# Performance work log

Hardware: AMD Instinct MI355X
Metric: run time of the kernel (lower is better)

Reference implementation:

```python
import jax, jax.numpy as jnp
import numpy as np

B = 32
NUM_CLASSES = 2


def _conv3d(x, w, b):
    # 3x3x3 'same' conv, NCDHW
    y = jax.lax.conv_general_dilated(x, w, (1, 1, 1), [(1, 1)] * 3,
                                     dimension_numbers=("NCDHW", "OIDHW", "NCDHW"))
    return y + b[None, :, None, None, None]


def _bn(x, g, b, axes, eps=1e-5):
    # training-mode batchnorm (biased variance), channel axis = 1
    m = jnp.mean(x, axes, keepdims=True)
    v = jnp.var(x, axes, keepdims=True)
    sh = [1] * x.ndim
    sh[1] = -1
    return (x - m) / jnp.sqrt(v + eps) * g.reshape(sh) + b.reshape(sh)


def _ln(x, g, b, eps=1e-6):
    m = jnp.mean(x, -1, keepdims=True)
    v = jnp.var(x, -1, keepdims=True)
    return (x - m) / jnp.sqrt(v + eps) * g + b


def _lin(x, w, b):
    return x @ w.T + b


def _conv1x1(x, w, b):
    # 1x1x1 Conv3d == channel-mixing linear
    return jnp.einsum("bcdhw,oc->bodhw", x, w) + b[None, :, None, None, None]


def _catnum(t, w, b, g, be, attr, out_attr):
    # Conv1d(attr->196, k=1) == Linear; BN1d over (batch, length); SiLU; tile channels
    t = _lin(t.reshape(t.shape[0], attr), w, b)               # [B,196]
    t = _bn(t[:, :, None], g, be, (0, 2))[:, :, 0]
    t = t * jax.nn.sigmoid(t)                                  # SiLU
    return jnp.broadcast_to(t.reshape(-1, 1, 4, 7, 7), (t.shape[0], out_attr, 4, 7, 7))


def _gcn(t, w, b):
    # all-pairs L1-distance affinity over CHANNELS (detached), then matmul + MLP + residual
    bsz, c = t.shape[0], t.shape[1]
    f = t.reshape(bsz, c, -1)                                  # [B,C,196]
    dist = jax.lax.stop_gradient(
        jnp.exp(-jnp.abs(f[:, :, None, :] - f[:, None, :, :]).sum(-1)))  # [B,C,C]
    out = jax.nn.relu(_lin(jnp.einsum("bij,bjn->bin", dist, f), w, b))
    return out.reshape(t.shape) + t


def _crossatt(img, text, e1_w, e1_b, e2_w, e2_b, f1_w, f1_b, f2_w, f2_b, f3_w, f3_b, f4_w, f4_b):
    # q/k/v each come from the SAME linear applied to the same input -> identical tensors
    iq = jax.nn.relu(_lin(img, e1_w, e1_b))                    # [B,128,196]
    tq = jax.nn.relu(_lin(text, e2_w, e2_b))                   # [B,45,196]
    att = lambda q, k: jax.nn.softmax(jnp.einsum("bik,bjk->bij", q, k), axis=-1)
    img_fea = att(iq, iq) @ iq
    text_fea = att(tq, tq) @ tq
    it_fea = att(iq, tq) @ tq
    ti_fea = att(tq, iq) @ iq
    return (_lin(img_fea, f1_w, f1_b) + _lin(it_fea, f3_w, f3_b) + img,
            _lin(text_fea, f2_w, f2_b) + _lin(ti_fea, f4_w, f4_b) + text)


def _cmsa(xf, w, b, fw, fb):
    # query=key=value (same conv applied thrice to same input)
    bsz, c, d, hh, ww = xf.shape
    q = jax.nn.relu(_conv1x1(xf, w, b)).reshape(bsz, c, -1)    # [B,173,196]
    A = jax.nn.softmax(jnp.einsum("bci,bcj->bij", q, q), axis=-1)  # [B,196,196]
    fea = jnp.einsum("bij,bcj->bci", A, q).reshape(bsz, c, d, hh, ww)
    return jax.nn.relu(_conv1x1(fea, fw, fb)) + xf


def _forward(x, oneHot, num, c1_w1, c1_b1, c1_g1, c1_be1, c1_w2, c1_b2, c1_g2, c1_be2,
             oh_w, oh_b, oh_g, oh_be, nm_w, nm_b, nm_g, nm_be,
             gm1_w, gm1_b, gm2_w, gm2_b, ln1_g, ln1_b, ln2_g, ln2_b,
             e1_w, e1_b, e2_w, e2_b, f1_w, f1_b, f2_w, f2_b, f3_w, f3_b, f4_w, f4_b,
             cm_w, cm_b, cmf_w, cmf_b, cls_w, cls_b):
    h = jax.nn.relu(_bn(_conv3d(x, c1_w1, c1_b1), c1_g1, c1_be1, (0, 2, 3, 4)))
    conv5 = jax.nn.relu(_bn(_conv3d(h, c1_w2, c1_b2), c1_g2, c1_be2, (0, 2, 3, 4)))  # [B,128,4,7,7]
    t_oh = _catnum(oneHot, oh_w, oh_b, oh_g, oh_be, 24, 30)    # [B,30,4,7,7]
    t_nm = _catnum(num, nm_w, nm_b, nm_g, nm_be, 11, 15)       # [B,15,4,7,7]
    text = jnp.concatenate([t_oh, t_nm], axis=1)               # [B,45,4,7,7]
    conv5 = _gcn(conv5, gm1_w, gm1_b)
    text = _gcn(text, gm2_w, gm2_b)
    bsz = x.shape[0]
    c5f = conv5.reshape(bsz, 128, 196)
    txf = text.reshape(bsz, 45, 196)
    ci, ct = _crossatt(_ln(c5f, ln1_g, ln1_b), _ln(txf, ln2_g, ln2_b),
                       e1_w, e1_b, e2_w, e2_b, f1_w, f1_b, f2_w, f2_b, f3_w, f3_b, f4_w, f4_b)
    feat = jnp.concatenate([(ci + c5f).reshape(bsz, 128, 4, 7, 7),
                            (ct + txf).reshape(bsz, 45, 4, 7, 7)], axis=1)  # [B,173,4,7,7]
    cmsa = _cmsa(feat, cm_w, cm_b, cmf_w, cmf_b)
    g1v = t_oh.reshape(bsz, 30, -1).sum(-1)
    g2v = t_nm.reshape(bsz, 15, -1).sum(-1)
    pcm = cmsa.reshape(bsz, 173, -1).sum(-1)
    return _lin(jnp.concatenate([g1v, g2v, pcm], axis=1), cls_w, cls_b)  # [B,num_classes]


def setup_inputs():
    key = jax.random.key(0)
    ks = iter(jax.random.split(key, 64))
    rn = lambda shape, s=0.02: jax.random.normal(next(ks), shape, jnp.float32) * s
    d = {}
    d["x"] = rn((B, 320, 4, 7, 7), 1.0)
    d["oneHot"] = (jax.random.uniform(next(ks), (B, 24)) > 0.5).astype(jnp.float32)
    d["num"] = rn((B, 11), 1.0)
    d["c1_w1"] = rn((128, 320, 3, 3, 3)); d["c1_b1"] = jnp.zeros(128)
    d["c1_g1"] = jnp.ones(128); d["c1_be1"] = jnp.zeros(128)
    d["c1_w2"] = rn((128, 128, 3, 3, 3)); d["c1_b2"] = jnp.zeros(128)
    d["c1_g2"] = jnp.ones(128); d["c1_be2"] = jnp.zeros(128)
    d["oh_w"] = rn((196, 24), 0.1); d["oh_b"] = jnp.zeros(196)
    d["oh_g"] = jnp.ones(196); d["oh_be"] = jnp.zeros(196)
    d["nm_w"] = rn((196, 11), 0.1); d["nm_b"] = jnp.zeros(196)
    d["nm_g"] = jnp.ones(196); d["nm_be"] = jnp.zeros(196)
    d["gm1_w"] = rn((196, 196), 0.05); d["gm1_b"] = jnp.zeros(196)
    d["gm2_w"] = rn((196, 196), 0.05); d["gm2_b"] = jnp.zeros(196)
    d["ln1_g"] = jnp.ones(196); d["ln1_b"] = jnp.zeros(196)
    d["ln2_g"] = jnp.ones(196); d["ln2_b"] = jnp.zeros(196)
    for n in ["e1", "e2", "f1", "f2", "f3", "f4"]:
        d[n + "_w"] = rn((196, 196), 0.05); d[n + "_b"] = jnp.zeros(196)
    d["cm_w"] = rn((173, 173), 0.05); d["cm_b"] = jnp.zeros(173)
    d["cmf_w"] = rn((173, 173), 0.05); d["cmf_b"] = jnp.zeros(173)
    d["cls_w"] = rn((NUM_CLASSES, 218), 0.05); d["cls_b"] = jnp.zeros(NUM_CLASSES)
    return d


def reference(x, oneHot, num, c1_w1, c1_b1, c1_g1, c1_be1, c1_w2, c1_b2, c1_g2, c1_be2,
              oh_w, oh_b, oh_g, oh_be, nm_w, nm_b, nm_g, nm_be,
              gm1_w, gm1_b, gm2_w, gm2_b, ln1_g, ln1_b, ln2_g, ln2_b,
              e1_w, e1_b, e2_w, e2_b, f1_w, f1_b, f2_w, f2_b, f3_w, f3_b, f4_w, f4_b,
              cm_w, cm_b, cmf_w, cmf_b, cls_w, cls_b):
    return _forward(x, oneHot, num, c1_w1, c1_b1, c1_g1, c1_be1, c1_w2, c1_b2, c1_g2, c1_be2,
                    oh_w, oh_b, oh_g, oh_be, nm_w, nm_b, nm_g, nm_be,
                    gm1_w, gm1_b, gm2_w, gm2_b, ln1_g, ln1_b, ln2_g, ln2_b,
                    e1_w, e1_b, e2_w, e2_b, f1_w, f1_b, f2_w, f2_b, f3_w, f3_b, f4_w, f4_b,
                    cm_w, cm_b, cmf_w, cmf_b, cls_w, cls_b)
```

## Files before the change

### kernel.cpp

```cpp
#include <hip/hip_runtime.h>
#include <hip/hip_bf16.h>


using bf16x8 = __attribute__((ext_vector_type(8))) short;
using f32x4  = __attribute__((ext_vector_type(4))) float;

typedef const __attribute__((address_space(1))) void gas_void;
typedef __attribute__((address_space(3))) void las_void;

__device__ __forceinline__ unsigned short f2bf(float f) {
    unsigned int u = __float_as_uint(f);
    u += 0x7FFFu + ((u >> 16) & 1u);
    return (unsigned short)(u >> 16);
}

__device__ __forceinline__ void d_wpack(const float* __restrict__ w,
                                        unsigned short* __restrict__ wp,
                                        int IC, int idx) {
    int nc = IC >> 3;
    if (idx >= 27 * 128 * nc) return;
    int c = idx % nc; int r = idx / nc; int oc = r & 127; int t = r >> 7;
    const float* ws = w + ((size_t)oc * IC + c * 8) * 27 + t;
    unsigned int o0 = f2bf(ws[0])   | ((unsigned int)f2bf(ws[27])  << 16);
    unsigned int o1 = f2bf(ws[54])  | ((unsigned int)f2bf(ws[81])  << 16);
    unsigned int o2 = f2bf(ws[108]) | ((unsigned int)f2bf(ws[135]) << 16);
    unsigned int o3 = f2bf(ws[162]) | ((unsigned int)f2bf(ws[189]) << 16);
    uint4 v; v.x = o0; v.y = o1; v.z = o2; v.w = o3;
    ((uint4*)wp)[idx] = v;
}

__device__ __forceinline__ void d_w173(const float* __restrict__ w,
                                       unsigned short* __restrict__ wb, int idx) {
    if (idx >= 176 * 192) return;
    int oc = idx / 192, c = idx - oc * 192;
    wb[idx] = (oc < 173 && c < 173) ? f2bf(w[(size_t)oc * 173 + c]) : (unsigned short)0;
}

__device__ __forceinline__ void d_wcat(const float* __restrict__ wA,
                                       const float* __restrict__ wB,
                                       unsigned short* __restrict__ outw, int idx) {
    if (idx >= 208 * 448) return;
    int n = idx / 448, k = idx - n * 448;
    unsigned short v = 0;
    if (n < 196) {
        if (k < 196) v = f2bf(wA[(size_t)n * 196 + k]);
        else if (k >= 224 && k < 420) v = f2bf(wB[(size_t)n * 196 + (k - 224)]);
    }
    outw[idx] = v;
}

__global__ void k_prep1(const float* __restrict__ c1w1, unsigned short* __restrict__ wp1,
                        const float* __restrict__ c1w2, unsigned short* __restrict__ wp2,
                        const float* __restrict__ x, unsigned short* __restrict__ xt1) {
    int blk = blockIdx.x, tid = threadIdx.x;
    if (blk < 540) { d_wpack(c1w1, wp1, 320, blk * 256 + tid); return; }
    blk -= 540;
    if (blk < 216) { d_wpack(c1w2, wp2, 128, blk * 256 + tid); return; }
    blk -= 216;
    int b = blk / 147, ib = blk - b * 147;
    const int tot = 5 * 208 * 36;
    int idx = ib * 256 + tid;
    if (idx >= tot) return;
    int g = idx / (208 * 36); int r2 = idx - g * (208 * 36);
    int s = r2 / 36, cp = r2 - s * 36;
    int cc = cp * 2;
    int ic = g * 64 + cc;
    unsigned int lo = 0, hi = 0;
    if (s < 196 && cc < 64 && ic < 320)         lo = f2bf(x[((size_t)b * 320 + ic) * 196 + s]);
    if (s < 196 && cc + 1 < 64 && ic + 1 < 320) hi = f2bf(x[((size_t)b * 320 + ic + 1) * 196 + s]);
    ((unsigned int*)xt1)[(size_t)b * tot + idx] = lo | (hi << 16);
}

__global__ void k_prep2(const float* __restrict__ cm_w, unsigned short* __restrict__ wcmb,
                        const float* __restrict__ cmf_w, unsigned short* __restrict__ wcmfb,
                        const float* __restrict__ gm1_w, unsigned short* __restrict__ gm1b,
                        float4* __restrict__ ftbz,
                        const float* __restrict__ gm2_w, const float* __restrict__ e1_w,
                        const float* __restrict__ e2_w, float* __restrict__ wT) {
    int blk = blockIdx.x, tid = threadIdx.x;
    if (blk < 132) { d_w173(cm_w, wcmb, blk * 256 + tid); return; }
    blk -= 132;
    if (blk < 132) { d_w173(cmf_w, wcmfb, blk * 256 + tid); return; }
    blk -= 132;
    if (blk < 182) {
        int idx = blk * 256 + tid;
        if (idx < 208 * 224) {
            int r = idx / 224, c = idx - r * 224;
            gm1b[idx] = (r < 196 && c < 196) ? f2bf(gm1_w[(size_t)r * 196 + c])
                                             : (unsigned short)0;
        }
        return;
    }
    blk -= 182;
    if (blk < 624) {
        int i = blk * 256 + tid;
        if (i < 159744) ftbz[i] = (float4){0.f, 0.f, 0.f, 0.f};
        return;
    }
    blk -= 624;
    {
        int m = blk / 196, i = blk - m * 196;
        const float* w = (m == 0) ? gm2_w : (m == 1) ? e1_w : e2_w;
        float* o = wT + (size_t)m * 38416;
        if (tid < 196) o[(size_t)i * 196 + tid] = w[(size_t)tid * 196 + i];
    }
}

__global__ void k_cattext(const float* __restrict__ oneHot, const float* __restrict__ num,
                          const float* __restrict__ ohw, const float* __restrict__ ohb,
                          const float* __restrict__ ohg, const float* __restrict__ ohbe,
                          const float* __restrict__ nmw, const float* __restrict__ nmb,
                          const float* __restrict__ nmg, const float* __restrict__ nmbe,
                          float* __restrict__ toh, float* __restrict__ tnm,
                          float* __restrict__ text, float* __restrict__ textT) {
    int blk = blockIdx.x;
    int lane = threadIdx.x;
    const int isOH = (blk < 196);
    const int j = isOH ? blk : blk - 196;
    const float* inp = isOH ? oneHot : num;
    const int A = isOH ? 24 : 11;
    const float* w = isOH ? ohw : nmw;
    const float* bias = isOH ? ohb : nmb;
    const float* g = isOH ? ohg : nmg;
    const float* be = isOH ? ohbe : nmbe;
    float v = 0.f;
    if (lane < 32) {
        v = bias[j];
        for (int k = 0; k < A; ++k) v += inp[lane * A + k] * w[j * A + k];
    }
    float s = (lane < 32) ? v : 0.f;
    float s2 = (lane < 32) ? v * v : 0.f;
    for (int m = 16; m; m >>= 1) { s += __shfl_xor(s, m, 32); s2 += __shfl_xor(s2, m, 32); }
    if (lane < 32) {
        float mean = s / 32.f;
        float var = s2 / 32.f - mean * mean;
        float rstd = rsqrtf(var + 1e-5f);
        float t = (v - mean) * rstd * g[j] + be[j];
        t = t / (1.f + expf(-t));
        int b = lane;
        if (isOH) {
            toh[b * 196 + j] = t;
            for (int c = 0; c < 30; ++c) {
                text[((size_t)(b * 45 + c)) * 196 + j] = t;
                textT[((size_t)(b * 196 + j)) * 45 + c] = t;
            }
        } else {
            tnm[b * 196 + j] = t;
            for (int c = 30; c < 45; ++c) {
                text[((size_t)(b * 45 + c)) * 196 + j] = t;
                textT[((size_t)(b * 196 + j)) * 45 + c] = t;
            }
        }
    }
}

__device__ __forceinline__ void d_dist_img(const float* __restrict__ f,
                                           const float* __restrict__ fT,
                                           unsigned short* __restrict__ distb,
                                           int bx, int b, int tid) {
    __shared__ float fi[4][196];
    const int i0 = bx * 4;
    for (int idx = tid; idx < 4 * 196; idx += 256) {
        int r = idx / 196, n = idx - r * 196;
        fi[r][n] = f[((size_t)(b * 128 + i0 + r)) * 196 + n];
    }
    __syncthreads();
    if (tid < 128) {
        const float* ft = fT + (size_t)b * 196 * 128 + tid;
        float a[4];
#pragma unroll
        for (int r = 0; r < 4; ++r) a[r] = 0.f;
#pragma unroll 4
        for (int n = 0; n < 196; ++n) {
            float v = ft[(size_t)n * 128];
#pragma unroll
            for (int r = 0; r < 4; ++r) a[r] += fabsf(fi[r][n] - v);
        }
#pragma unroll
        for (int r = 0; r < 4; ++r)
            distb[((size_t)(b * 128 + i0 + r)) * 128 + tid] = f2bf(expf(-a[r]));
    }
}

__device__ __forceinline__ void d_dist_txt(const float* __restrict__ f,
                                           const float* __restrict__ fT,
                                           float* __restrict__ dist,
                                           int bx, int b, int tid) {
    __shared__ float fi2[3][196];
    const int i0 = bx * 3;
    for (int idx = tid; idx < 3 * 196; idx += 256) {
        int r = idx / 196, n = idx - r * 196;
        fi2[r][n] = f[((size_t)(b * 45 + i0 + r)) * 196 + n];
    }
    __syncthreads();
    if (tid < 45) {
        const float* ft = fT + (size_t)b * 196 * 45 + tid;
        float a[3];
#pragma unroll
        for (int r = 0; r < 3; ++r) a[r] = 0.f;
#pragma unroll 4
        for (int n = 0; n < 196; ++n) {
            float v = ft[(size_t)n * 45];
#pragma unroll
            for (int r = 0; r < 3; ++r) a[r] += fabsf(fi2[r][n] - v);
        }
#pragma unroll
        for (int r = 0; r < 3; ++r)
            dist[((size_t)(b * 45 + i0 + r)) * 45 + tid] = expf(-a[r]);
    }
}

__global__ void k_dist_both(const float* __restrict__ fimg, const float* __restrict__ fTimg,
                            unsigned short* __restrict__ distb,
                            const float* __restrict__ ftxt, const float* __restrict__ fTtxt,
                            float* __restrict__ dist2) {
    int blk = blockIdx.x, tid = threadIdx.x;
    if (blk < 1024) d_dist_img(fimg, fTimg, distb, blk & 31, blk >> 5, tid);
    else { int r = blk - 1024; d_dist_txt(ftxt, fTtxt, dist2, r % 15, r / 15, tid); }
}

__global__ void k_prep3(float4* __restrict__ tqz,
                        const float* __restrict__ f1w, const float* __restrict__ f3w,
                        unsigned short* __restrict__ wcI,
                        const float* __restrict__ f4w, const float* __restrict__ f2w,
                        unsigned short* __restrict__ wcT) {
    int blk = blockIdx.x, tid = threadIdx.x;
    if (blk < 208) {
        int i = blk * 256 + tid;
        if (i < 53248) tqz[i] = (float4){0.f, 0.f, 0.f, 0.f};
        return;
    }
    blk -= 208;
    if (blk < 364) { d_wcat(f1w, f3w, wcI, blk * 256 + tid); return; }
    blk -= 364;
    d_wcat(f4w, f2w, wcT, blk * 256 + tid);
}

__global__ void k_prep4(float4* __restrict__ zA, float4* __restrict__ zB) {
    int blk = blockIdx.x, tid = threadIdx.x;
    if (blk < 1344) {
        int i = blk * 256 + tid;
        if (i < 344064) zA[i] = (float4){0.f, 0.f, 0.f, 0.f};
        return;
    }
    blk -= 1344;
    int i = blk * 256 + tid;
    if (i < 319488) zB[i] = (float4){0.f, 0.f, 0.f, 0.f};
}

template <int IC, int G, int NT, int NH>
__global__ __launch_bounds__(256, 3) void k_convchunk4(
    const unsigned short* __restrict__ xt, const unsigned short* __restrict__ wp,
    float* __restrict__ part) {
    __shared__ unsigned short xs[208 * 72];
    __shared__ char bbuf[2][NT * 2048];
    const int tid = threadIdx.x;
    const int bx = blockIdx.x, b = blockIdx.y;
    const int mh = bx & 1;
    const int nh = (bx >> 1) % NH;
    const int g  = (bx >> 1) / NH;
    const int w = tid >> 6, l = tid & 63;

    {
        const bf16x8* s8 = (const bf16x8*)(xt + ((size_t)b * G + g) * (208 * 72));
        bf16x8* d8 = (bf16x8*)xs;
        for (int c = tid; c < 208 * 72 / 8; c += 256) d8[c] = s8[c];
    }

    const char* wslice = (const char*)wp +
                         ((size_t)(nh * NT * 16) * IC + (size_t)g * 64) * 2;
    auto stageB = [&](int t) {
        char* dst = &bbuf[t & 1][w * (NT * 512)];
        const char* wt_ = wslice + (size_t)t * 128 * IC * 2;
#pragma unroll
        for (int c = 0; c < NT / 2; ++c) {
            int q = w * (NT * 512) + c * 1024 + l * 16;
            int row = q >> 7, col = q & 127;
            int scol = col ^ ((row & 7) << 4);
            gas_void* src = (gas_void*)(wt_ + (size_t)row * IC * 2 + scol);
            __builtin_amdgcn_global_load_lds(src, (las_void*)(dst + c * 1024),
                                             16, 0, 0);
        }
    };

    const int lane = tid & 63;
    const int a = lane & 15, kg = lane >> 4;

    int md[2], mhh[2], mw[2];
#pragma unroll
    for (int i = 0; i < 2; ++i) {
        int m = (mh * 8 + (tid >> 6) * 2 + i) * 16 + a;
        md[i] = m / 49; int rr = m - md[i] * 49;
        mhh[i] = rr / 7; mw[i] = rr - mhh[i] * 7;
    }

    f32x4 acc[2][NT];
#pragma unroll
    for (int i = 0; i < 2; ++i)
#pragma unroll
        for (int nt = 0; nt < NT; ++nt) acc[i][nt] = (f32x4){0.f, 0.f, 0.f, 0.f};

    const bf16x8 zv = {0, 0, 0, 0, 0, 0, 0, 0};

    stageB(0);
    __syncthreads();

    for (int t = 0; t < 27; ++t) {
        if (t < 26) stageB(t + 1);
        const int kd = t / 9, kh = (t / 3) % 3, kw = t % 3;
        int rsrc[2]; bool ok[2];
#pragma unroll
        for (int i = 0; i < 2; ++i) {
            int d2 = md[i] + kd - 1, h2 = mhh[i] + kh - 1, w2 = mw[i] + kw - 1;
            ok[i] = ((unsigned)d2 < 4u) & ((unsigned)h2 < 7u) & ((unsigned)w2 < 7u);
            rsrc[i] = ok[i] ? (d2 * 49 + h2 * 7 + w2) : 0;
        }
        bf16x8 A[2][2];
#pragma unroll
        for (int kk = 0; kk < 2; ++kk)
#pragma unroll
            for (int i = 0; i < 2; ++i) {
                bf16x8 v = *(const bf16x8*)(xs + rsrc[i] * 72 + kk * 32 + kg * 8);
                A[kk][i] = ok[i] ? v : zv;
            }
        const char* bb = &bbuf[t & 1][0];
#pragma unroll
        for (int kk = 0; kk < 2; ++kk)
#pragma unroll
            for (int nt = 0; nt < NT; ++nt) {
                int row = nt * 16 + a;
                int cb = (kk * 64 + kg * 16) ^ ((row & 7) << 4);
                bf16x8 B = *(const bf16x8*)(bb + row * 128 + cb);
#pragma unroll
                for (int i = 0; i < 2; ++i)
                    acc[i][nt] = __builtin_amdgcn_mfma_f32_16x16x32_bf16(
                        A[kk][i], B, acc[i][nt], 0, 0, 0);
            }
        __syncthreads();
    }

    float* dst = part + ((size_t)g * 32 + b) * (128 * 196);
#pragma unroll
    for (int i = 0; i < 2; ++i) {
        int m0 = (mh * 8 + (tid >> 6) * 2 + i) * 16 + kg * 4;
        if (m0 < 196) {
#pragma unroll
            for (int nt = 0; nt < NT; ++nt) {
                int oc = nh * NT * 16 + nt * 16 + a;
                *(f32x4*)(dst + (size_t)oc * 196 + m0) = acc[i][nt];
            }
        }
    }
}

template <int G, int C>
__global__ void k_reduce_stats(const float* __restrict__ part, float* __restrict__ y,
                               float* __restrict__ pst) {
    const int ch = blockIdx.x, b = blockIdx.y;
    const int tid = threadIdx.x;
    __shared__ float r1[4], r2[4];
    float v = 0.f;
    if (tid < 196) {
#pragma unroll
        for (int g = 0; g < G; ++g)
            v += part[((size_t)(g * 32 + b) * C + ch) * 196 + tid];
        y[((size_t)b * C + ch) * 196 + tid] = v;
    }
    float s = v, s2 = v * v;
    for (int sh = 32; sh; sh >>= 1) { s += __shfl_xor(s, sh); s2 += __shfl_xor(s2, sh); }
    if ((tid & 63) == 0) { r1[tid >> 6] = s; r2[tid >> 6] = s2; }
    __syncthreads();
    if (tid == 0) {
        pst[(ch * 32 + b) * 2]     = r1[0] + r1[1] + r1[2] + r1[3];
        pst[(ch * 32 + b) * 2 + 1] = r2[0] + r2[1] + r2[2] + r2[3];
    }
}

__global__ void k_bn_apply2(float* __restrict__ y, const float* __restrict__ pst,
                            const float* __restrict__ g, const float* __restrict__ be,
                            float* __restrict__ fT, unsigned short* __restrict__ fTb,
                            unsigned short* __restrict__ xtc, int C) {
    int idx = blockIdx.x;
    int ch = idx % C, b = idx / C;
    int s = threadIdx.x;
    float S = 0.f, S2 = 0.f;
    for (int b2 = 0; b2 < 32; ++b2) {
        S += pst[(ch * 32 + b2) * 2];
        S2 += pst[(ch * 32 + b2) * 2 + 1];
    }
    if (s < 196) {
        float m = S / 6272.f;
        float r = rsqrtf(S2 / 6272.f - m * m + 1e-5f);
        float v = y[(size_t)idx * 196 + s];
        float o = fmaxf((v - m) * r * g[ch] + be[ch], 0.f);
        y[(size_t)idx * 196 + s] = o;
        if (fT) fT[((size_t)b * 196 + s) * C + ch] = o;
        if (fTb) fTb[((size_t)b * 208 + s) * C + ch] = f2bf(o);
        if (xtc) {
            int G = C >> 6, gch = ch >> 6, cc = ch & 63;
            xtc[(((size_t)b * G + gch) * 208 + s) * 72 + cc] = f2bf(o);
        }
    }
}

template <int MROWS, int MTILES, int KP, int KK, int EPI, int NS>
__global__ __launch_bounds__(256, 2) void k_bgemm(
    const unsigned short* __restrict__ Ab, size_t ABS,
    const unsigned short* __restrict__ Bb, size_t BBS,
    const float* __restrict__ bias,
    unsigned short* __restrict__ p0, unsigned short* __restrict__ p1,
    const float* __restrict__ resid, float* __restrict__ outf) {
    constexpr int KPS = KP + 8;
    __shared__ unsigned short xsA[64 * KPS];
    __shared__ char bbuf[2][208 * 64];
    const int tid = threadIdx.x, bx = blockIdx.x, b = blockIdx.y;
    const int wv = tid >> 6, lane = tid & 63, a = lane & 15, kg = lane >> 4;
    const int nh = bx % NS, mg = bx / NS;
    const int NT0 = (NS == 1) ? 0 : nh * 7;
    const int NTN = (NS == 1) ? 13 : ((nh == 0) ? 7 : 6);

    const unsigned short* Abase = Ab + (size_t)b * ABS;
    {
        const int rowu = KP / 2;
        for (int i = tid; i < 64 * rowu; i += 256) {
            int r = i / rowu, cu = i - r * rowu;
            int gr = mg * 64 + r; if (gr > MROWS - 1) gr = MROWS - 1;
            unsigned int v = ((const unsigned int*)(Abase + (size_t)gr * KP))[cu];
            *(unsigned int*)&xsA[r * KPS + cu * 2] = v;
        }
    }
    const char* Bbase = (const char*)(Bb + (size_t)b * BBS);
    auto stageB = [&](int kk) {
        char* dst0 = &bbuf[kk & 1][0];
        const int cnt = NTN * 64;
#pragma unroll
        for (int c = 0; c < 4; ++c) {
            int idx = tid + c * 256;
            if (idx < cnt) {
                int lrow = idx >> 2, u = idx & 3;
                int grow = NT0 * 16 + lrow;
                gas_void* src = (gas_void*)(Bbase + (size_t)grow * (KP * 2) +
                                            kk * 64 + u * 16);
                __builtin_amdgcn_global_load_lds(src, (las_void*)(dst0 + (size_t)idx * 16),
                                                 16, 0, 0);
            }
        }
    };

    int mt = mg * 4 + wv; if (mt > MTILES - 1) mt = MTILES - 1;
    const int arow = mt * 16 + a - mg * 64;

    f32x4 acc[13];
#pragma unroll
    for (int nt = 0; nt < 13; ++nt) acc[nt] = (f32x4){0.f, 0.f, 0.f, 0.f};

    stageB(0);
    __syncthreads();
    for (int kk = 0; kk < KK; ++kk) {
        if (kk + 1 < KK) stageB(kk + 1);
        bf16x8 Af = *(const bf16x8*)&xsA[arow * KPS + kk * 32 + kg * 8];
        const char* bb = &bbuf[kk & 1][0];
#pragma unroll
        for (int nt = 0; nt < 13; ++nt) {
            if (nt >= NT0 && nt < NT0 + NTN) {
                bf16x8 Bf = *(const bf16x8*)(bb + ((nt - NT0) * 16 + a) * 64 + kg * 16);
                acc[nt] = __builtin_amdgcn_mfma_f32_16x16x32_bf16(Af, Bf, acc[nt], 0, 0, 0);
            }
        }
        __syncthreads();
    }

    const int mbase = mt * 16 + kg * 4;
    if (EPI == 0) {
#pragma unroll
        for (int nt = 0; nt < 13; ++nt) {
            if (nt < NT0 || nt >= NT0 + NTN) continue;
            int col = nt * 16 + a;
            if (col < 196) {
#pragma unroll
                for (int j = 0; j < 4; ++j) {
                    int row = mbase + j;
                    if (row < 173) {
                        unsigned short h = f2bf(fmaxf(acc[nt][j] + bias[row], 0.f));
                        p0[((size_t)b * 176 + row) * 224 + col] = h;
                        p1[((size_t)b * 208 + col) * 192 + row] = h;
                    }
                }
            }
        }
    } else if (EPI == 1) {
#pragma unroll
        for (int j = 0; j < 4; ++j) {
            int row = mbase + j;
            float m = -3.4e38f;
#pragma unroll
            for (int nt = 0; nt < 13; ++nt) {
                int col = nt * 16 + a;
                float s = (col < 196) ? acc[nt][j] : -3.4e38f;
                m = fmaxf(m, s);
            }
            for (int msk = 1; msk < 16; msk <<= 1) m = fmaxf(m, __shfl_xor(m, msk));
            float e[13]; float sum = 0.f;
#pragma unroll
            for (int nt = 0; nt < 13; ++nt) {
                int col = nt * 16 + a;
                float v = (col < 196) ? expf(acc[nt][j] - m) : 0.f;
                e[nt] = v; sum += v;
            }
            for (int msk = 1; msk < 16; msk <<= 1) sum += __shfl_xor(sum, msk);
            float inv = 1.f / sum;
            if (row < 196) {
#pragma unroll
                for (int nt = 0; nt < 13; ++nt) {
                    int col = nt * 16 + a;
                    p0[((size_t)b * 208 + row) * 224 + col] = f2bf(e[nt] * inv);
                }
            }
        }
    } else if (EPI == 2) {
#pragma unroll
        for (int nt = 0; nt < 13; ++nt) {
            if (nt < NT0 || nt >= NT0 + NTN) continue;
            int col = nt * 16 + a;
#pragma unroll
            for (int j = 0; j < 4; ++j) {
                int row = mbase + j;
                if (row < 173)
                    p0[((size_t)b * 208 + col) * 192 + row] = f2bf(acc[nt][j]);
            }
        }
    } else if (EPI == 3) {
#pragma unroll
        for (int nt = 0; nt < 13; ++nt) {
            if (nt < NT0 || nt >= NT0 + NTN) continue;
            int col = nt * 16 + a;
            if (col < 196) {
#pragma unroll
                for (int j = 0; j < 4; ++j) {
                    int row = mbase + j;
                    if (row < 173) {
                        size_t rr = ((size_t)b * 173 + row) * 196 + col;
                        outf[rr] = fmaxf(acc[nt][j] + bias[row], 0.f) + resid[rr];
                    }
                }
            }
        }
    } else {
#pragma unroll
        for (int nt = 0; nt < 13; ++nt) {
            if (nt < NT0 || nt >= NT0 + NTN) continue;
            int col = nt * 16 + a;
            if (col < 196) {
#pragma unroll
                for (int j = 0; j < 4; ++j) {
                    int row = mbase + j;
                    size_t rr = ((size_t)b * 128 + row) * 196 + col;
                    outf[rr] = fmaxf(acc[nt][j] + bias[col], 0.f) + resid[rr];
                }
            }
        }
    }
}

__global__ __launch_bounds__(256, 2) void k_gcnpair(
    const unsigned short* __restrict__ distb, const unsigned short* __restrict__ fTb,
    unsigned short* __restrict__ tmpb,
    const float* __restrict__ d2, const float* __restrict__ t1,
    const float* __restrict__ gm2T, const float* __restrict__ gm2b,
    float* __restrict__ t3) {
    __shared__ unsigned short xsA[64 * 136];
    __shared__ char bbuf[2][208 * 64];
    __shared__ float ds[3][45];
    __shared__ float ts[3][196];
    const int tid = threadIdx.x, b = blockIdx.y;
    int bx = blockIdx.x;
    if (bx < 4) {
        const int wv = tid >> 6, lane = tid & 63, a = lane & 15, kg = lane >> 4;
        const int nh = bx % 2, mg = bx / 2;
        const int NT0 = nh * 7, NTN = (nh == 0) ? 7 : 6;
        const unsigned short* Abase = distb + (size_t)b * 128 * 128;
        for (int i = tid; i < 64 * 64; i += 256) {
            int r = i / 64, cu = i - r * 64;
            int gr = mg * 64 + r;
            unsigned int v = ((const unsigned int*)(Abase + (size_t)gr * 128))[cu];
            *(unsigned int*)&xsA[r * 136 + cu * 2] = v;
        }
        const char* Bbase = (const char*)(fTb + (size_t)b * 208 * 128);
        auto stageB = [&](int kk) {
            char* dst0 = &bbuf[kk & 1][0];
            const int cnt = NTN * 64;
#pragma unroll
            for (int c = 0; c < 4; ++c) {
                int idx = tid + c * 256;
                if (idx < cnt) {
                    int lrow = idx >> 2, u = idx & 3;
                    int grow = NT0 * 16 + lrow;
                    gas_void* src = (gas_void*)(Bbase + (size_t)grow * 256 +
                                                kk * 64 + u * 16);
                    __builtin_amdgcn_global_load_lds(src,
                        (las_void*)(dst0 + (size_t)idx * 16), 16, 0, 0);
                }
            }
        };
        int mt = mg * 4 + wv;
        const int arow = mt * 16 + a - mg * 64;
        f32x4 acc[13];
#pragma unroll
        for (int nt = 0; nt < 13; ++nt) acc[nt] = (f32x4){0.f, 0.f, 0.f, 0.f};
        stageB(0);
        __syncthreads();
        for (int kk = 0; kk < 4; ++kk) {
            if (kk + 1 < 4) stageB(kk + 1);
            bf16x8 Af = *(const bf16x8*)&xsA[arow * 136 + kk * 32 + kg * 8];
            const char* bb = &bbuf[kk & 1][0];
#pragma unroll
            for (int nt = 0; nt < 13; ++nt) {
                if (nt >= NT0 && nt < NT0 + NTN) {
                    bf16x8 Bf = *(const bf16x8*)(bb + ((nt - NT0) * 16 + a) * 64 + kg * 16);
                    acc[nt] = __builtin_amdgcn_mfma_f32_16x16x32_bf16(Af, Bf, acc[nt], 0, 0, 0);
                }
            }
            __syncthreads();
        }
        const int mbase = mt * 16 + kg * 4;
#pragma unroll
        for (int nt = 0; nt < 13; ++nt) {
            if (nt < NT0 || nt >= NT0 + NTN) continue;
            int col = nt * 16 + a;
#pragma unroll
            for (int j = 0; j < 4; ++j) {
                int row = mbase + j;
                unsigned short h = (col < 196) ? f2bf(acc[nt][j]) : (unsigned short)0;
                tmpb[((size_t)b * 128 + row) * 224 + col] = h;
            }
        }
    } else {
        const int i0 = (bx - 4) * 3;
        for (int idx = tid; idx < 3 * 45; idx += 256) {
            int r = idx / 45, j = idx - r * 45;
            ds[r][j] = d2[((size_t)(b * 45 + i0 + r)) * 45 + j];
        }
        __syncthreads();
        if (tid < 196) {
            float a[3];
#pragma unroll
            for (int r = 0; r < 3; ++r) a[r] = 0.f;
#pragma unroll 4
            for (int j = 0; j < 45; ++j) {
                float v = t1[((size_t)b * 45 + j) * 196 + tid];
#pragma unroll
                for (int r = 0; r < 3; ++r) a[r] += ds[r][j] * v;
            }
#pragma unroll
            for (int r = 0; r < 3; ++r) ts[r][tid] = a[r];
        }
        __syncthreads();
        if (tid < 196) {
            float a[3];
            float bi = gm2b[tid];
#pragma unroll
            for (int r = 0; r < 3; ++r) a[r] = bi;
#pragma unroll 4
            for (int n = 0; n < 196; ++n) {
                float wv = gm2T[(size_t)n * 196 + tid];
#pragma unroll
                for (int r = 0; r < 3; ++r) a[r] += ts[r][n] * wv;
            }
#pragma unroll
            for (int r = 0; r < 3; ++r) {
                size_t rr = ((size_t)(b * 45 + i0 + r)) * 196 + tid;
                t3[rr] = fmaxf(a[r], 0.f) + t1[rr];
            }
        }
    }
}

struct AG {
    const unsigned short* Ab; unsigned long ABS;
    const unsigned short* Bb; unsigned long BBS;
    const float* biasA; const float* biasB;
    const float* lnres; const float* res2;
    unsigned short* p0; unsigned long p0rs, p0bs;
    float* feat; unsigned short* ftb; int cbase;
    int MROWS; int MTILES;
};

template <int KPA, int KPB, int KK, int EPI, int STAGEA, int NS>
__global__ __launch_bounds__(256, 2) void k_agemm2(AG pa, AG pc, int split) {
    constexpr int KPS = KPA + 8;
    __shared__ unsigned short xsA[STAGEA ? 64 * KPS : 64];
    __shared__ char bbuf[2][208 * 64];
    const AG P = (blockIdx.x < split) ? pa : pc;
    const int bx = (blockIdx.x < split) ? blockIdx.x : blockIdx.x - split;
    const int tid = threadIdx.x, b = blockIdx.y;
    const int wv = tid >> 6, lane = tid & 63, a = lane & 15, kg = lane >> 4;
    const int nh = bx % NS, mg = bx / NS;
    const int NT0 = (NS == 1) ? 0 : nh * 7;
    const int NTN = (NS == 1) ? 13 : ((nh == 0) ? 7 : 6);
    const int MROWS = P.MROWS, MTILES = P.MTILES;

    const unsigned short* Abase = P.Ab + (size_t)b * P.ABS;
    if (STAGEA) {
        const int rowu = KPA / 2;
        for (int i = tid; i < 64 * rowu; i += 256) {
            int r = i / rowu, cu = i - r * rowu;
            int gr = mg * 64 + r; if (gr > MROWS - 1) gr = MROWS - 1;
            unsigned int v = ((const unsigned int*)(Abase + (size_t)gr * KPA))[cu];
            *(unsigned int*)&xsA[r * KPS + cu * 2] = v;
        }
    }
    const char* Bbase = (const char*)(P.Bb + (size_t)b * P.BBS);
    auto stageB = [&](int kk) {
        char* dst0 = &bbuf[kk & 1][0];
        const int cnt = NTN * 64;
#pragma unroll
        for (int c = 0; c < 4; ++c) {
            int idx = tid + c * 256;
            if (idx < cnt) {
                int lrow = idx >> 2, u = idx & 3;
                int grow = NT0 * 16 + lrow;
                gas_void* src = (gas_void*)(Bbase + (size_t)grow * (KPB * 2) +
                                            kk * 64 + u * 16);
                __builtin_amdgcn_global_load_lds(src, (las_void*)(dst0 + (size_t)idx * 16),
                                                 16, 0, 0);
            }
        }
    };

    int mt = mg * 4 + wv; if (mt > MTILES - 1) mt = MTILES - 1;

    f32x4 acc[13];
#pragma unroll
    for (int nt = 0; nt < 13; ++nt) acc[nt] = (f32x4){0.f, 0.f, 0.f, 0.f};

    stageB(0);
    __syncthreads();
    for (int kk = 0; kk < KK; ++kk) {
        if (kk + 1 < KK) stageB(kk + 1);
        bf16x8 Af;
        if (STAGEA) {
            int arow = mt * 16 + a - mg * 64;
            Af = *(const bf16x8*)&xsA[arow * KPS + kk * 32 + kg * 8];
        } else {
            int gr = mt * 16 + a; if (gr > MROWS - 1) gr = MROWS - 1;
            Af = *(const bf16x8*)(Abase + (size_t)gr * KPA + kk * 32 + kg * 8);
        }
        const char* bb = &bbuf[kk & 1][0];
#pragma unroll
        for (int nt = 0; nt < 13; ++nt) {
            if (nt >= NT0 && nt < NT0 + NTN) {
                bf16x8 Bf = *(const bf16x8*)(bb + ((nt - NT0) * 16 + a) * 64 + kg * 16);
                acc[nt] = __builtin_amdgcn_mfma_f32_16x16x32_bf16(Af, Bf, acc[nt], 0, 0, 0);
            }
        }
        __syncthreads();
    }

    const int mbase = mt * 16 + kg * 4;
    if (EPI == 5) {
#pragma unroll
        for (int j = 0; j < 4; ++j) {
            int row = mbase + j;
            float mA = -3.4e38f, mB = -3.4e38f;
#pragma unroll
            for (int nt = 0; nt < 8; ++nt) mA = fmaxf(mA, acc[nt][j]);
#pragma unroll
            for (int nt = 8; nt < 13; ++nt) {
                int col = nt * 16 + a;
                float s = (col < 173) ? acc[nt][j] : -3.4e38f;
                mB = fmaxf(mB, s);
            }
            for (int msk = 1; msk < 16; msk <<= 1) {
                mA = fmaxf(mA, __shfl_xor(mA, msk));
                mB = fmaxf(mB, __shfl_xor(mB, msk));
            }
            float eA[8], eB[5];
            float sA = 0.f, sB = 0.f;
#pragma unroll
            for (int nt = 0; nt < 8; ++nt) { eA[nt] = expf(acc[nt][j] - mA); sA += eA[nt]; }
#pragma unroll
            for (int nt = 8; nt < 13; ++nt) {
                int col = nt * 16 + a;
                float v = (col < 173) ? expf(acc[nt][j] - mB) : 0.f;
                eB[nt - 8] = v; sB += v;
            }
            for (int msk = 1; msk < 16; msk <<= 1) {
                sA += __shfl_xor(sA, msk);
                sB += __shfl_xor(sB, msk);
            }
            float iA = 1.f / sA, iB = 1.f / sB;
            if (row < MROWS) {
#pragma unroll
                for (int nt = 0; nt < 12; ++nt) {
                    int col = nt * 16 + a;
                    float v = (nt < 8) ? eA[nt] * iA
                                       : ((col < 173) ? eB[nt - 8] * iB : 0.f);
                    P.p0[(size_t)b * P.p0bs + (size_t)row * P.p0rs + col] = f2bf(v);
                }
            }
        }
    } else {
#pragma unroll
        for (int nt = 0; nt < 13; ++nt) {
            if (nt < NT0 || nt >= NT0 + NTN) continue;
            int col = nt * 16 + a;
            if (col < 196) {
#pragma unroll
                for (int j = 0; j < 4; ++j) {
                    int row = mbase + j;
                    if (row < MROWS) {
                        size_t rr = ((size_t)b * MROWS + row) * 196 + col;
                        float v = acc[nt][j] + P.biasA[col] + P.biasB[col] +
                                  P.lnres[rr] + P.res2[rr];
                        P.feat[((size_t)b * 173 + P.cbase + row) * 196 + col] = v;
                        P.ftb[((size_t)(b * 208 + col)) * 192 + P.cbase + row] = f2bf(v);
                    }
                }
            }
        }
    }
}

struct PVP { const unsigned short* P; unsigned long Pbs;
             unsigned short* F; unsigned long Fbs; int MROWS; int MTILES; };

__global__ __launch_bounds__(256, 2) void k_pv2(
    PVP pa, PVP pc, int split,
    const unsigned short* __restrict__ V1, unsigned long V1bs,
    const unsigned short* __restrict__ V2, unsigned long V2bs) {
    constexpr int KPS = 200;
    __shared__ unsigned short xsA[64 * KPS];
    __shared__ char bbuf[2][208 * 64];
    const PVP P = (blockIdx.x < split) ? pa : pc;
    const int bx = (blockIdx.x < split) ? blockIdx.x : blockIdx.x - split;
    const int tid = threadIdx.x, b = blockIdx.y;
    const int wv = tid >> 6, lane = tid & 63, a = lane & 15, kg = lane >> 4;
    const int nh = bx % 2, mg = bx / 2;
    const int NT0 = nh * 7, NTN = (nh == 0) ? 7 : 6;
    const int MROWS = P.MROWS, MTILES = P.MTILES;

    const unsigned short* Abase = P.P + (size_t)b * P.Pbs;
    {
        for (int i = tid; i < 64 * 96; i += 256) {
            int r = i / 96, cu = i - r * 96;
            int gr = mg * 64 + r; if (gr > MROWS - 1) gr = MROWS - 1;
            unsigned int v = ((const unsigned int*)(Abase + (size_t)gr * 192))[cu];
            *(unsigned int*)&xsA[r * KPS + cu * 2] = v;
        }
    }
    int mt = mg * 4 + wv; if (mt > MTILES - 1) mt = MTILES - 1;
    const int arow = mt * 16 + a - mg * 64;
    const int mbase = mt * 16 + kg * 4;

    auto run = [&](const unsigned short* Vb, size_t Vbs_, int KPB, int KK,
                   int AOFFe, int outoff) {
        f32x4 acc[13];
#pragma unroll
        for (int nt = 0; nt < 13; ++nt) acc[nt] = (f32x4){0.f, 0.f, 0.f, 0.f};
        const char* Bbase = (const char*)(Vb + (size_t)b * Vbs_);
        auto stageB = [&](int kk) {
            char* dst0 = &bbuf[kk & 1][0];
            const int cnt = NTN * 64;
#pragma unroll
            for (int c = 0; c < 4; ++c) {
                int idx = tid + c * 256;
                if (idx < cnt) {
                    int lrow = idx >> 2, u = idx & 3;
                    int grow = NT0 * 16 + lrow;
                    gas_void* src = (gas_void*)(Bbase + (size_t)grow * (KPB * 2) +
                                                kk * 64 + u * 16);
                    __builtin_amdgcn_global_load_lds(src,
                        (las_void*)(dst0 + (size_t)idx * 16), 16, 0, 0);
                }
            }
        };
        stageB(0);
        __syncthreads();
        for (int kk = 0; kk < KK; ++kk) {
            if (kk + 1 < KK) stageB(kk + 1);
            bf16x8 Af = *(const bf16x8*)&xsA[arow * KPS + AOFFe + kk * 32 + kg * 8];
            const char* bb = &bbuf[kk & 1][0];
#pragma unroll
            for (int nt = 0; nt < 13; ++nt) {
                if (nt >= NT0 && nt < NT0 + NTN) {
                    bf16x8 Bf = *(const bf16x8*)(bb + ((nt - NT0) * 16 + a) * 64 + kg * 16);
                    acc[nt] = __builtin_amdgcn_mfma_f32_16x16x32_bf16(Af, Bf, acc[nt], 0, 0, 0);
                }
            }
            __syncthreads();
        }
#pragma unroll
        for (int nt = 0; nt < 13; ++nt) {
            if (nt < NT0 || nt >= NT0 + NTN) continue;
            int col = nt * 16 + a;
#pragma unroll
            for (int j = 0; j < 4; ++j) {
                int row = mbase + j;
                if (row < MROWS) {
                    unsigned short h = (col < 196) ? f2bf(acc[nt][j]) : (unsigned short)0;
                    P.F[(size_t)b * P.Fbs + (size_t)row * 448 + outoff + col] = h;
                }
            }
        }
        if (nh == 1) {
            int col = 208 + a;
#pragma unroll
            for (int j = 0; j < 4; ++j) {
                int row = mbase + j;
                if (row < MROWS)
                    P.F[(size_t)b * P.Fbs + (size_t)row * 448 + outoff + col] = 0;
            }
        }
    };
    run(V1, V1bs, 128, 4, 0, 0);
    run(V2, V2bs, 64, 2, 128, 224);
}

template <int R, int ROWS, int KOFF, int TS>
__device__ __forceinline__ void d_lnlin(const float* __restrict__ x,
                                        const float* __restrict__ g,
                                        const float* __restrict__ be,
                                        const float* __restrict__ eT,
                                        const float* __restrict__ eb,
                                        float* __restrict__ lnout,
                                        unsigned short* __restrict__ kcat,
                                        unsigned short* __restrict__ tbuf,
                                        int bx, int b) {
    __shared__ float ls[ROWS][196];
    const int i0 = bx * ROWS;
    const int tid = threadIdx.x;
    const int wv = tid >> 6, lane = tid & 63;
    for (int idx = tid; idx < ROWS * 196; idx += 256) {
        int r = idx / 196, n = idx - r * 196;
        ls[r][n] = x[((size_t)(b * R + i0 + r)) * 196 + n];
    }
    __syncthreads();
    for (int k = 0;; ++k) {
        int r = wv + 4 * k;
        if (r >= ROWS) break;
        float s = 0.f, s2 = 0.f;
        for (int j = lane; j < 196; j += 64) { float v = ls[r][j]; s += v; s2 += v * v; }
        for (int sh = 32; sh; sh >>= 1) { s += __shfl_xor(s, sh); s2 += __shfl_xor(s2, sh); }
        float mean = s / 196.f;
        float var = s2 / 196.f - mean * mean;
        float rstd = rsqrtf(var + 1e-6f);
        size_t rowo = ((size_t)(b * R + i0 + r)) * 196;
        for (int j = lane; j < 196; j += 64) {
            float l = (ls[r][j] - mean) * rstd * g[j] + be[j];
            ls[r][j] = l;
            lnout[rowo + j] = l;
        }
    }
    __syncthreads();
    if (tid < 224) {
        float a[ROWS];
        if (tid < 196) {
            float bi = eb[tid];
#pragma unroll
            for (int r = 0; r < ROWS; ++r) a[r] = bi;
#pragma unroll 4
            for (int n = 0; n < 196; ++n) {
                float ev = eT[(size_t)n * 196 + tid];
#pragma unroll
                for (int r = 0; r < ROWS; ++r) a[r] += ls[r][n] * ev;
            }
        }
#pragma unroll
        for (int r = 0; r < ROWS; ++r) {
            unsigned short h = 0;
            if (tid < 196) h = f2bf(fmaxf(a[r], 0.f));
            kcat[((size_t)(b * 208 + KOFF + i0 + r)) * 224 + tid] = h;
            if (tid < 196) tbuf[((size_t)(b * 208 + tid)) * TS + (i0 + r)] = h;
        }
    }
}

__global__ void k_lnlin_both(const float* __restrict__ ximg, const float* __restrict__ g1,
                             const float* __restrict__ b1, const float* __restrict__ e1T,
                             const float* __restrict__ e1b, float* __restrict__ ln1out,
                             const float* __restrict__ xtxt, const float* __restrict__ g2,
                             const float* __restrict__ b2, const float* __restrict__ e2T,
                             const float* __restrict__ e2b, float* __restrict__ ln2out,
                             unsigned short* __restrict__ kcat,
                             unsigned short* __restrict__ iqT,
                             unsigned short* __restrict__ tqT) {
    int blk = blockIdx.x;
    if (blk < 1024)
        d_lnlin<128, 4, 0, 128>(ximg, g1, b1, e1T, e1b, ln1out, kcat, iqT,
                                blk & 31, blk >> 5);
    else {
        int r = blk - 1024;
        d_lnlin<45, 3, 128, 64>(xtxt, g2, b2, e2T, e2b, ln2out, kcat, tqT,
                                r % 15, r / 15);
    }
}

__global__ void k_finale(const float* __restrict__ toh, const float* __restrict__ tnm,
                         const float* __restrict__ cms, const float* __restrict__ cls_w,
                         const float* __restrict__ cls_b, float* __restrict__ out) {
    int b = blockIdx.x;
    __shared__ float pcm[173];
    __shared__ float r1[4], r2[4];
    int tid = threadIdx.x;
    float a = (tid < 196) ? toh[b * 196 + tid] : 0.f;
    float c = (tid < 196) ? tnm[b * 196 + tid] : 0.f;
    for (int sh = 32; sh; sh >>= 1) { a += __shfl_xor(a, sh); c += __shfl_xor(c, sh); }
    if ((tid & 63) == 0) { r1[tid >> 6] = a; r2[tid >> 6] = c; }
    if (tid < 173) {
        float s = 0.f;
        const float* p = &cms[((size_t)b * 173 + tid) * 196];
        for (int n = 0; n < 196; ++n) s += p[n];
        pcm[tid] = s;
    }
    __syncthreads();
    if (tid < 2) {
        float soh = r1[0] + r1[1] + r1[2] + r1[3];
        float snm = r2[0] + r2[1] + r2[2] + r2[3];
        const float* wrow = &cls_w[tid * 218];
        float acc = cls_b[tid];
        float w1 = 0.f, w2 = 0.f;
        for (int k = 0; k < 30; ++k) w1 += wrow[k];
        for (int k = 30; k < 45; ++k) w2 += wrow[k];
        acc += soh * w1 + snm * w2;
        for (int k = 0; k < 173; ++k) acc += wrow[45 + k] * pcm[k];
        out[b * 2 + tid] = acc;
    }
}

extern "C" void kernel_launch(void* const* d_in, const int* in_sizes, int n_in,
                              void* d_out, int out_size, void* d_ws, size_t ws_size,
                              hipStream_t stream) {
    const float* x      = (const float*)d_in[0];
    const float* oneHot = (const float*)d_in[1];
    const float* num    = (const float*)d_in[2];
    const float* c1_w1  = (const float*)d_in[3];
    const float* c1_g1  = (const float*)d_in[5];
    const float* c1_be1 = (const float*)d_in[6];
    const float* c1_w2  = (const float*)d_in[7];
    const float* c1_g2  = (const float*)d_in[9];
    const float* c1_be2 = (const float*)d_in[10];
    const float* oh_w   = (const float*)d_in[11];
    const float* oh_b   = (const float*)d_in[12];
    const float* oh_g   = (const float*)d_in[13];
    const float* oh_be  = (const float*)d_in[14];
    const float* nm_w   = (const float*)d_in[15];
    const float* nm_b   = (const float*)d_in[16];
    const float* nm_g   = (const float*)d_in[17];
    const float* nm_be  = (const float*)d_in[18];
    const float* gm1_w  = (const float*)d_in[19];
    const float* gm1_b  = (const float*)d_in[20];
    const float* gm2_w  = (const float*)d_in[21];
    const float* gm2_b  = (const float*)d_in[22];
    const float* ln1_g  = (const float*)d_in[23];
    const float* ln1_b  = (const float*)d_in[24];
    const float* ln2_g  = (const float*)d_in[25];
    const float* ln2_b  = (const float*)d_in[26];
    const float* e1_w   = (const float*)d_in[27];
    const float* e1_b   = (const float*)d_in[28];
    const float* e2_w   = (const float*)d_in[29];
    const float* e2_b   = (const float*)d_in[30];
    const float* f1_w   = (const float*)d_in[31];
    const float* f1_b   = (const float*)d_in[32];
    const float* f2_w   = (const float*)d_in[33];
    const float* f2_b   = (const float*)d_in[34];
    const float* f3_w   = (const float*)d_in[35];
    const float* f3_b   = (const float*)d_in[36];
    const float* f4_w   = (const float*)d_in[37];
    const float* f4_b   = (const float*)d_in[38];
    const float* cm_w   = (const float*)d_in[39];
    const float* cm_b   = (const float*)d_in[40];
    const float* cmf_w  = (const float*)d_in[41];
    const float* cmf_b  = (const float*)d_in[42];
    const float* cls_w  = (const float*)d_in[43];
    const float* cls_b  = (const float*)d_in[44];
    float* out = (float*)d_out;
    float* W = (float*)d_ws;

    const size_t L = 802816;
    const size_t T = 282240;
    const size_t F3 = 1085056;
    const size_t o_A    = 0;
    const size_t o_B    = L;
    const size_t o_C    = 2 * L;
    const size_t o_Kcat = 3 * L;
    const size_t o_iqT  = o_Kcat + 745472;
    const size_t o_t1   = 4 * L + T;
    const size_t o_t3   = 4 * L + 2 * T;
    const size_t o_ln2  = 4 * L + 3 * T;
    const size_t o_toh  = 4 * L + 4 * T;
    const size_t o_tnm  = o_toh + 6272;
    const size_t o_st   = o_tnm + 6272;
    const size_t o_wT   = o_st + 1024;
    const size_t o_feat = o_wT + 8 * 38416;
    const size_t o_q    = o_feat + F3;
    const size_t o_Fimg = o_q;
    const size_t o_dd   = o_q + F3;
    const size_t o_db   = o_dd;
    const size_t o_d2   = o_dd + 524288;
    const size_t o_gm1b = o_dd + 589088;
    const size_t o_fTb  = o_dd + 612384;
    const size_t o_tqT  = o_dd;
    const size_t o_wcI  = o_dd + 212992;
    const size_t o_wcT  = o_wcI + 46592;
    const size_t o_pbf  = o_dd;
    const size_t o_qbf  = o_dd + 745472;
    const size_t o_Ftxt = o_qbf;
    const size_t o_wcm  = o_qbf + 630784;
    const size_t o_wcmf = o_wcm + 16896;
    const size_t o_ftb  = o_wcmf + 16896;
    const size_t o_tr   = o_ftb + 638976;
    const size_t o_Pimg = o_tr;
    const size_t o_Ptxt = o_tr + 393216;
    const size_t o_qtb  = o_tr;
    const size_t o_ps   = 10158208;
    const size_t o_xt1 = o_dd;
    const size_t o_xt2 = o_xt1 + 1198080;
    const size_t o_wp1 = o_xt2 + 479232;
    const size_t o_wp2 = o_wp1 + 552960;

    float* part = W + 3 * L;
    unsigned short* xt1 = (unsigned short*)(W + o_xt1);
    unsigned short* xt2 = (unsigned short*)(W + o_xt2);
    unsigned short* wp1 = (unsigned short*)(W + o_wp1);
    unsigned short* wp2 = (unsigned short*)(W + o_wp2);
    unsigned short* kcatb = (unsigned short*)(W + o_Kcat);
    unsigned short* iqTb = (unsigned short*)(W + o_iqT);
    unsigned short* tqTb = (unsigned short*)(W + o_tqT);
    unsigned short* wcatI = (unsigned short*)(W + o_wcI);
    unsigned short* wcatT = (unsigned short*)(W + o_wcT);
    unsigned short* Fimg = (unsigned short*)(W + o_Fimg);
    unsigned short* Ftxt = (unsigned short*)(W + o_Ftxt);
    unsigned short* Pimg = (unsigned short*)(W + o_Pimg);
    unsigned short* Ptxt = (unsigned short*)(W + o_Ptxt);
    unsigned short* ftb = (unsigned short*)(W + o_ftb);
    unsigned short* qtb = (unsigned short*)(W + o_qtb);
    unsigned short* feab = (unsigned short*)(W + o_qtb + 638976);
    unsigned short* qbf = (unsigned short*)(W + o_qbf);
    unsigned short* wcmb = (unsigned short*)(W + o_wcm);
    unsigned short* wcmfb = (unsigned short*)(W + o_wcmf);
    unsigned short* pbf = (unsigned short*)(W + o_pbf);
    unsigned short* distb = (unsigned short*)(W + o_db);
    unsigned short* gm1b = (unsigned short*)(W + o_gm1b);
    unsigned short* fTb = (unsigned short*)(W + o_fTb);
    unsigned short* tmpb = (unsigned short*)(W + o_A);
    float* gm2T = W + o_wT + 0 * 38416;
    float* e1T  = W + o_wT + 1 * 38416;
    float* e2T  = W + o_wT + 2 * 38416;

    k_prep1<<<5460, 256, 0, stream>>>(c1_w1, wp1, c1_w2, wp2, x, xt1);

    k_convchunk4<320, 5, 4, 2><<<dim3(20, 32), 256, 0, stream>>>(xt1, wp1, part);
    k_reduce_stats<5, 128><<<dim3(128, 32), 256, 0, stream>>>(part, W + o_A, W + o_ps);
    k_bn_apply2<<<4096, 256, 0, stream>>>(W + o_A, W + o_ps, c1_g1, c1_be1,
                                          nullptr, nullptr, xt2, 128);

    k_convchunk4<128, 2, 2, 4><<<dim3(16, 32), 256, 0, stream>>>(xt2, wp2, part);
    k_reduce_stats<2, 128><<<dim3(128, 32), 256, 0, stream>>>(part, W + o_B,
                                                              W + o_ps + 8192);
    k_bn_apply2<<<4096, 256, 0, stream>>>(W + o_B, W + o_ps + 8192, c1_g2, c1_be2,
                                          W + o_tr, fTb, nullptr, 128);

    k_prep2<<<1658, 256, 0, stream>>>(cm_w, wcmb, cmf_w, wcmfb, gm1_w, gm1b,
                                      (float4*)(W + o_ftb), gm2_w, e1_w, e2_w, W + o_wT);

    k_cattext<<<392, 64, 0, stream>>>(oneHot, num, oh_w, oh_b, oh_g, oh_be,
                                      nm_w, nm_b, nm_g, nm_be,
                                      W + o_toh, W + o_tnm, W + o_t1, W + o_tr + L);

    k_dist_both<<<1504, 256, 0, stream>>>(W + o_B, W + o_tr, distb,
                                          W + o_t1, W + o_tr + L, W + o_d2);

    k_gcnpair<<<dim3(19, 32), 256, 0, stream>>>(distb, fTb, tmpb,
                                                W + o_d2, W + o_t1, gm2T, gm2_b,
                                                W + o_t3);

    k_bgemm<128, 8, 224, 7, 8, 2><<<dim3(4, 32), 256, 0, stream>>>(
        tmpb, (size_t)128 * 224, gm1b, 0, gm1_b,
        nullptr, nullptr, W + o_B, W + o_C);

    k_prep3<<<936, 256, 0, stream>>>((float4*)(W + o_tqT), f1_w, f3_w, wcatI,
                                     f4_w, f2_w, wcatT);

    k_lnlin_both<<<1504, 256, 0, stream>>>(W + o_C, ln1_g, ln1_b, e1T, e1_b, W + o_B,
                                           W + o_t3, ln2_g, ln2_b, e2T, e2_b, W + o_ln2,
                                           kcatb, iqTb, tqTb);

    {
        AG a{}, c{};
        a.Ab = kcatb; a.ABS = 208 * 224; a.Bb = kcatb; a.BBS = 208 * 224;
        a.p0 = Pimg; a.p0rs = 192; a.p0bs = (unsigned long)128 * 192;
        a.MROWS = 128; a.MTILES = 8;
        c = a;
        c.Ab = kcatb + 128 * 224; c.p0 = Ptxt; c.p0bs = (unsigned long)48 * 192;
        c.MROWS = 45; c.MTILES = 3;
        k_agemm2<224, 224, 7, 5, 1, 1><<<dim3(3, 32), 256, 0, stream>>>(a, c, 2);
    }

    {
        PVP a{Pimg, (unsigned long)128 * 192, Fimg, (unsigned long)128 * 448, 128, 8};
        PVP c{Ptxt, (unsigned long)48 * 192, Ftxt, (unsigned long)48 * 448, 45, 3};
        k_pv2<<<dim3(6, 32), 256, 0, stream>>>(a, c, 4, iqTb, (unsigned long)208 * 128,
                                               tqTb, (unsigned long)208 * 64);
    }

    {
        AG a{}, c{};
        a.Ab = Fimg; a.ABS = (unsigned long)128 * 448; a.Bb = wcatI; a.BBS = 0;
        a.biasA = f1_b; a.biasB = f3_b; a.lnres = W + o_B; a.res2 = W + o_C;
        a.feat = W + o_feat; a.ftb = ftb; a.cbase = 0; a.MROWS = 128; a.MTILES = 8;
        c = a;
        c.Ab = Ftxt; c.ABS = (unsigned long)48 * 448; c.Bb = wcatT;
        c.biasA = f2_b; c.biasB = f4_b; c.lnres = W + o_ln2; c.res2 = W + o_t3;
        c.cbase = 128; c.MROWS = 45; c.MTILES = 3;
        k_agemm2<448, 448, 14, 4, 0, 2><<<dim3(6, 32), 256, 0, stream>>>(a, c, 4);
    }

    k_prep4<<<2592, 256, 0, stream>>>((float4*)(W + o_pbf), (float4*)(W + o_qtb));

    k_bgemm<176, 11, 192, 6, 0, 2><<<dim3(6, 32), 256, 0, stream>>>(
        wcmb, 0, ftb, (size_t)208 * 192, cm_b, qbf, qtb, nullptr, nullptr);
    k_bgemm<208, 13, 192, 6, 1, 1><<<dim3(4, 32), 256, 0, stream>>>(
        qtb, (size_t)208 * 192, qtb, (size_t)208 * 192, nullptr, pbf, nullptr,
        nullptr, nullptr);
    k_bgemm<176, 11, 224, 7, 2, 2><<<dim3(6, 32), 256, 0, stream>>>(
        qbf, (size_t)176 * 224, pbf, (size_t)208 * 224, nullptr, feab, nullptr,
        nullptr, nullptr);
    k_bgemm<176, 11, 192, 6, 3, 2><<<dim3(6, 32), 256, 0, stream>>>(
        wcmfb, 0, feab, (size_t)208 * 192, cmf_b, nullptr, nullptr,
        W + o_feat, W + o_q);

    k_finale<<<32, 256, 0, stream>>>(W + o_toh, W + o_tnm, W + o_q, cls_w, cls_b, out);
}
```

Measured before the change: 317.9 us.

## Fuse attention score/softmax with PV GEMM and merge small prep kernels

Replaces the separate score GEMM (k_agemm2 with softmax epilogue) and PV kernel (k_pv2) with a single k_attn kernel. It keeps the softmax probabilities in LDS instead of writing them to global memory and reading them back. It also folds k_cattext into k_prep2 and the gcn final GEMM plus k_prep3 into one k_gcnfin launch, which cuts launch count and inter-kernel gaps. The risk is that k_attn uses only 96 blocks with no N-split, so parallelism per launch drops.

```diff
diff --git a/kernel.cpp b/kernel.cpp
--- a/kernel.cpp
+++ b/kernel.cpp
@@ -47,6 +47,54 @@
         else if (k >= 224 && k < 420) v = f2bf(wB[(size_t)n * 196 + (k - 224)]);
     }
     outw[idx] = v;
+}
+
+__device__ __forceinline__ void d_cattext(
+    int idx, int lane,
+    const float* __restrict__ oneHot, const float* __restrict__ num,
+    const float* __restrict__ ohw, const float* __restrict__ ohb,
+    const float* __restrict__ ohg, const float* __restrict__ ohbe,
+    const float* __restrict__ nmw, const float* __restrict__ nmb,
+    const float* __restrict__ nmg, const float* __restrict__ nmbe,
+    float* __restrict__ toh, float* __restrict__ tnm,
+    float* __restrict__ text, float* __restrict__ textT) {
+    const int isOH = (idx < 196);
+    const int j = isOH ? idx : idx - 196;
+    const float* inp = isOH ? oneHot : num;
+    const int A = isOH ? 24 : 11;
+    const float* w = isOH ? ohw : nmw;
+    const float* bias = isOH ? ohb : nmb;
+    const float* g = isOH ? ohg : nmg;
+    const float* be = isOH ? ohbe : nmbe;
+    float v = 0.f;
+    if (lane < 32) {
+        v = bias[j];
+        for (int k = 0; k < A; ++k) v += inp[lane * A + k] * w[j * A + k];
+    }
+    float s = (lane < 32) ? v : 0.f;
+    float s2 = (lane < 32) ? v * v : 0.f;
+    for (int m = 16; m; m >>= 1) { s += __shfl_xor(s, m, 32); s2 += __shfl_xor(s2, m, 32); }
+    if (lane < 32) {
+        float mean = s / 32.f;
+        float var = s2 / 32.f - mean * mean;
+        float rstd = rsqrtf(var + 1e-5f);
+        float t = (v - mean) * rstd * g[j] + be[j];
+        t = t / (1.f + expf(-t));
+        int b = lane;
+        if (isOH) {
+            toh[b * 196 + j] = t;
+            for (int c = 0; c < 30; ++c) {
+                text[((size_t)(b * 45 + c)) * 196 + j] = t;
+                textT[((size_t)(b * 196 + j)) * 45 + c] = t;
+            }
+        } else {
+            tnm[b * 196 + j] = t;
+            for (int c = 30; c < 45; ++c) {
+                text[((size_t)(b * 45 + c)) * 196 + j] = t;
+                textT[((size_t)(b * 196 + j)) * 45 + c] = t;
+            }
+        }
+    }
 }
 
 __global__ void k_prep1(const float* __restrict__ c1w1, unsigned short* __restrict__ wp1,
@@ -76,7 +124,14 @@
                         const float* __restrict__ gm1_w, unsigned short* __restrict__ gm1b,
                         float4* __restrict__ ftbz,
                         const float* __restrict__ gm2_w, const float* __restrict__ e1_w,
-                        const float* __restrict__ e2_w, float* __restrict__ wT) {
+                        const float* __restrict__ e2_w, float* __restrict__ wT,
+                        const float* __restrict__ oneHot, const float* __restrict__ num,
+                        const float* __restrict__ ohw, const float* __restrict__ ohb,
+                        const float* __restrict__ ohg, const float* __restrict__ ohbe,
+                        const float* __restrict__ nmw, const float* __restrict__ nmb,
+                        const float* __restrict__ nmg, const float* __restrict__ nmbe,
+                        float* __restrict__ toh, float* __restrict__ tnm,
+                        float* __restrict__ text, float* __restrict__ textT) {
     int blk = blockIdx.x, tid = threadIdx.x;
     if (blk < 132) { d_w173(cm_w, wcmb, blk * 256 + tid); return; }
     blk -= 132;
@@ -98,59 +153,19 @@
         return;
     }
     blk -= 624;
-    {
+    if (blk < 588) {
         int m = blk / 196, i = blk - m * 196;
         const float* w = (m == 0) ? gm2_w : (m == 1) ? e1_w : e2_w;
         float* o = wT + (size_t)m * 38416;
         if (tid < 196) o[(size_t)i * 196 + tid] = w[(size_t)tid * 196 + i];
-    }
-}
-
-__global__ void k_cattext(const float* __restrict__ oneHot, const float* __restrict__ num,
-                          const float* __restrict__ ohw, const float* __restrict__ ohb,
-                          const float* __restrict__ ohg, const float* __restrict__ ohbe,
-                          const float* __restrict__ nmw, const float* __restrict__ nmb,
-                          const float* __restrict__ nmg, const float* __restrict__ nmbe,
-                          float* __restrict__ toh, float* __restrict__ tnm,
-                          float* __restrict__ text, float* __restrict__ textT) {
-    int blk = blockIdx.x;
-    int lane = threadIdx.x;
-    const int isOH = (blk < 196);
-    const int j = isOH ? blk : blk - 196;
-    const float* inp = isOH ? oneHot : num;
-    const int A = isOH ? 24 : 11;
-    const float* w = isOH ? ohw : nmw;
-    const float* bias = isOH ? ohb : nmb;
-    const float* g = isOH ? ohg : nmg;
-    const float* be = isOH ? ohbe : nmbe;
-    float v = 0.f;
-    if (lane < 32) {
-        v = bias[j];
-        for (int k = 0; k < A; ++k) v += inp[lane * A + k] * w[j * A + k];
-    }
-    float s = (lane < 32) ? v : 0.f;
-    float s2 = (lane < 32) ? v * v : 0.f;
-    for (int m = 16; m; m >>= 1) { s += __shfl_xor(s, m, 32); s2 += __shfl_xor(s2, m, 32); }
-    if (lane < 32) {
-        float mean = s / 32.f;
-        float var = s2 / 32.f - mean * mean;
-        float rstd = rsqrtf(var + 1e-5f);
-        float t = (v - mean) * rstd * g[j] + be[j];
-        t = t / (1.f + expf(-t));
-        int b = lane;
-        if (isOH) {
-            toh[b * 196 + j] = t;
-            for (int c = 0; c < 30; ++c) {
-                text[((size_t)(b * 45 + c)) * 196 + j] = t;
-                textT[((size_t)(b * 196 + j)) * 45 + c] = t;
-            }
-        } else {
-            tnm[b * 196 + j] = t;
-            for (int c = 30; c < 45; ++c) {
-                text[((size_t)(b * 45 + c)) * 196 + j] = t;
-                textT[((size_t)(b * 196 + j)) * 45 + c] = t;
-            }
-        }
+        return;
+    }
+    blk -= 588;
+    {
+        int idx = blk * 4 + (tid >> 6);
+        if (idx < 392)
+            d_cattext(idx, tid & 63, oneHot, num, ohw, ohb, ohg, ohbe,
+                      nmw, nmb, nmg, nmbe, toh, tnm, text, textT);
     }
 }
 
@@ -217,23 +232,6 @@
     int blk = blockIdx.x, tid = threadIdx.x;
     if (blk < 1024) d_dist_img(fimg, fTimg, distb, blk & 31, blk >> 5, tid);
     else { int r = blk - 1024; d_dist_txt(ftxt, fTtxt, dist2, r % 15, r / 15, tid); }
-}
-
-__global__ void k_prep3(float4* __restrict__ tqz,
-                        const float* __restrict__ f1w, const float* __restrict__ f3w,
-                        unsigned short* __restrict__ wcI,
-                        const float* __restrict__ f4w, const float* __restrict__ f2w,
-                        unsigned short* __restrict__ wcT) {
-    int blk = blockIdx.x, tid = threadIdx.x;
-    if (blk < 208) {
-        int i = blk * 256 + tid;
-        if (i < 53248) tqz[i] = (float4){0.f, 0.f, 0.f, 0.f};
-        return;
-    }
-    blk -= 208;
-    if (blk < 364) { d_wcat(f1w, f3w, wcI, blk * 256 + tid); return; }
-    blk -= 364;
-    d_wcat(f4w, f2w, wcT, blk * 256 + tid);
 }
 
 __global__ void k_prep4(float4* __restrict__ zA, float4* __restrict__ zB) {
@@ -529,7 +527,7 @@
                     p0[((size_t)b * 208 + col) * 192 + row] = f2bf(acc[nt][j]);
             }
         }
-    } else if (EPI == 3) {
+    } else {
 #pragma unroll
         for (int nt = 0; nt < 13; ++nt) {
             if (nt < NT0 || nt >= NT0 + NTN) continue;
@@ -542,20 +540,6 @@
                         size_t rr = ((size_t)b * 173 + row) * 196 + col;
                         outf[rr] = fmaxf(acc[nt][j] + bias[row], 0.f) + resid[rr];
                     }
-                }
-            }
-        }
-    } else {
-#pragma unroll
-        for (int nt = 0; nt < 13; ++nt) {
-            if (nt < NT0 || nt >= NT0 + NTN) continue;
-            int col = nt * 16 + a;
-            if (col < 196) {
-#pragma unroll
-                for (int j = 0; j < 4; ++j) {
-                    int row = mbase + j;
-                    size_t rr = ((size_t)b * 128 + row) * 196 + col;
-                    outf[rr] = fmaxf(acc[nt][j] + bias[col], 0.f) + resid[rr];
                 }
             }
         }
@@ -675,21 +659,268 @@
     }
 }
 
+__global__ __launch_bounds__(256, 2) void k_gcnfin(
+    const unsigned short* __restrict__ tmpb, const unsigned short* __restrict__ gm1b,
+    const float* __restrict__ gm1bias, const float* __restrict__ resid,
+    float* __restrict__ outf,
+    float4* __restrict__ tqz,
+    const float* __restrict__ f1w, const float* __restrict__ f3w,
+    unsigned short* __restrict__ wcI,
+    const float* __restrict__ f4w, const float* __restrict__ f2w,
+    unsigned short* __restrict__ wcT) {
+    __shared__ unsigned short xsA[64 * 232];
+    __shared__ char bbuf[2][208 * 64];
+    const int tid = threadIdx.x;
+    int blk = blockIdx.x;
+    if (blk < 128) {
+        const int b = blk >> 2, bx = blk & 3;
+        const int wv = tid >> 6, lane = tid & 63, a = lane & 15, kg = lane >> 4;
+        const int nh = bx & 1, mg = bx >> 1;
+        const int NT0 = nh * 7, NTN = (nh == 0) ? 7 : 6;
+        const unsigned short* Abase = tmpb + (size_t)b * (128 * 224);
+        for (int i = tid; i < 64 * 112; i += 256) {
+            int r = i / 112, cu = i - r * 112;
+            int gr = mg * 64 + r;
+            unsigned int v = ((const unsigned int*)(Abase + (size_t)gr * 224))[cu];
+            *(unsigned int*)&xsA[r * 232 + cu * 2] = v;
+        }
+        auto stageB = [&](int kk) {
+            char* dst0 = &bbuf[kk & 1][0];
+            const int cnt = NTN * 64;
+#pragma unroll
+            for (int c = 0; c < 4; ++c) {
+                int idx = tid + c * 256;
+                if (idx < cnt) {
+                    int lrow = idx >> 2, u = idx & 3;
+                    int grow = NT0 * 16 + lrow;
+                    gas_void* src = (gas_void*)((const char*)gm1b + (size_t)grow * 448 +
+                                                kk * 64 + u * 16);
+                    __builtin_amdgcn_global_load_lds(src,
+                        (las_void*)(dst0 + (size_t)idx * 16), 16, 0, 0);
+                }
+            }
+        };
+        int mt = mg * 4 + wv;
+        const int arow = mt * 16 + a - mg * 64;
+        f32x4 acc[13];
+#pragma unroll
+        for (int nt = 0; nt < 13; ++nt) acc[nt] = (f32x4){0.f, 0.f, 0.f, 0.f};
+        stageB(0);
+        __syncthreads();
+        for (int kk = 0; kk < 7; ++kk) {
+            if (kk + 1 < 7) stageB(kk + 1);
+            bf16x8 Af = *(const bf16x8*)&xsA[arow * 232 + kk * 32 + kg * 8];
+            const char* bb = &bbuf[kk & 1][0];
+#pragma unroll
+            for (int nt = 0; nt < 13; ++nt) {
+                if (nt >= NT0 && nt < NT0 + NTN) {
+                    bf16x8 Bf = *(const bf16x8*)(bb + ((nt - NT0) * 16 + a) * 64 + kg * 16);
+                    acc[nt] = __builtin_amdgcn_mfma_f32_16x16x32_bf16(Af, Bf, acc[nt], 0, 0, 0);
+                }
+            }
+            __syncthreads();
+        }
+        const int mbase = mt * 16 + kg * 4;
+#pragma unroll
+        for (int nt = 0; nt < 13; ++nt) {
+            if (nt < NT0 || nt >= NT0 + NTN) continue;
+            int col = nt * 16 + a;
+            if (col < 196) {
+#pragma unroll
+                for (int j = 0; j < 4; ++j) {
+                    int row = mbase + j;
+                    size_t rr = ((size_t)b * 128 + row) * 196 + col;
+                    outf[rr] = fmaxf(acc[nt][j] + gm1bias[col], 0.f) + resid[rr];
+                }
+            }
+        }
+    } else {
+        blk -= 128;
+        if (blk < 208) {
+            int i = blk * 256 + tid;
+            if (i < 53248) tqz[i] = (float4){0.f, 0.f, 0.f, 0.f};
+            return;
+        }
+        blk -= 208;
+        if (blk < 364) { d_wcat(f1w, f3w, wcI, blk * 256 + tid); return; }
+        blk -= 364;
+        d_wcat(f4w, f2w, wcT, blk * 256 + tid);
+    }
+}
+
+__global__ __launch_bounds__(256, 2) void k_attn(
+    const unsigned short* __restrict__ kcatb,
+    const unsigned short* __restrict__ V1, const unsigned short* __restrict__ V2,
+    unsigned short* __restrict__ Fimg, unsigned short* __restrict__ Ftxt) {
+    __shared__ unsigned short xsA[64 * 232];
+    __shared__ char bbuf[2][208 * 64];
+    const int tid = threadIdx.x;
+    const int blk = blockIdx.x;
+    const int b = blk / 3, m = blk - b * 3;
+    const int isTxt = (m == 2);
+    const int mg = isTxt ? 0 : m;
+    const int MROWS = isTxt ? 45 : 128;
+    const int MTILES = isTxt ? 3 : 8;
+    const unsigned short* Abase = kcatb + (size_t)b * (208 * 224) + (isTxt ? 128 * 224 : 0);
+    unsigned short* F = isTxt ? Ftxt + (size_t)b * (48 * 448)
+                              : Fimg + (size_t)b * (128 * 448);
+    const int wv = tid >> 6, lane = tid & 63, a = lane & 15, kg = lane >> 4;
+
+    for (int i = tid; i < 64 * 112; i += 256) {
+        int r = i / 112, cu = i - r * 112;
+        int gr = mg * 64 + r; if (gr > MROWS - 1) gr = MROWS - 1;
+        unsigned int v = ((const unsigned int*)(Abase + (size_t)gr * 224))[cu];
+        *(unsigned int*)&xsA[r * 232 + cu * 2] = v;
+    }
+    const char* Bs = (const char*)(kcatb + (size_t)b * (208 * 224));
+    auto stageBs = [&](int kk) {
+        char* dst0 = &bbuf[kk & 1][0];
+#pragma unroll
+        for (int c = 0; c < 4; ++c) {
+            int idx = tid + c * 256;
+            if (idx < 832) {
+                int lrow = idx >> 2, u = idx & 3;
+                gas_void* src = (gas_void*)(Bs + (size_t)lrow * 448 + kk * 64 + u * 16);
+                __builtin_amdgcn_global_load_lds(src,
+                    (las_void*)(dst0 + (size_t)idx * 16), 16, 0, 0);
+            }
+        }
+    };
+    int mt = mg * 4 + wv; if (mt > MTILES - 1) mt = MTILES - 1;
+    const int arow0 = mt * 16 + a - mg * 64;
+    const int mbase = mt * 16 + kg * 4;
+
+    f32x4 acc[13];
+#pragma unroll
+    for (int nt = 0; nt < 13; ++nt) acc[nt] = (f32x4){0.f, 0.f, 0.f, 0.f};
+    stageBs(0);
+    __syncthreads();
+    for (int kk = 0; kk < 7; ++kk) {
+        if (kk + 1 < 7) stageBs(kk + 1);
+        bf16x8 Af = *(const bf16x8*)&xsA[arow0 * 232 + kk * 32 + kg * 8];
+        const char* bb = &bbuf[kk & 1][0];
+#pragma unroll
+        for (int nt = 0; nt < 13; ++nt) {
+            bf16x8 Bf = *(const bf16x8*)(bb + (nt * 16 + a) * 64 + kg * 16);
+            acc[nt] = __builtin_amdgcn_mfma_f32_16x16x32_bf16(Af, Bf, acc[nt], 0, 0, 0);
+        }
+        __syncthreads();
+    }
+
+    unsigned short* xsP = xsA;
+#pragma unroll
+    for (int j = 0; j < 4; ++j) {
+        float mA = -3.4e38f, mB = -3.4e38f;
+#pragma unroll
+        for (int nt = 0; nt < 8; ++nt) mA = fmaxf(mA, acc[nt][j]);
+#pragma unroll
+        for (int nt = 8; nt < 13; ++nt) {
+            int col = nt * 16 + a;
+            float s = (col < 173) ? acc[nt][j] : -3.4e38f;
+            mB = fmaxf(mB, s);
+        }
+        for (int msk = 1; msk < 16; msk <<= 1) {
+            mA = fmaxf(mA, __shfl_xor(mA, msk));
+            mB = fmaxf(mB, __shfl_xor(mB, msk));
+        }
+        float eA[8], eB[5];
+        float sA = 0.f, sB = 0.f;
+#pragma unroll
+        for (int nt = 0; nt < 8; ++nt) { eA[nt] = expf(acc[nt][j] - mA); sA += eA[nt]; }
+#pragma unroll
+        for (int nt = 8; nt < 13; ++nt) {
+            int col = nt * 16 + a;
+            float v = (col < 173) ? expf(acc[nt][j] - mB) : 0.f;
+            eB[nt - 8] = v; sB += v;
+        }
+        for (int msk = 1; msk < 16; msk <<= 1) {
+            sA += __shfl_xor(sA, msk);
+            sB += __shfl_xor(sB, msk);
+        }
+        float iA = 1.f / sA, iB = 1.f / sB;
+        int lrow = mbase + j - mg * 64;
+#pragma unroll
+        for (int nt = 0; nt < 12; ++nt) {
+            int col = nt * 16 + a;
+            float v = (nt < 8) ? eA[nt] * iA : ((col < 173) ? eB[nt - 8] * iB : 0.f);
+            xsP[lrow * 200 + col] = f2bf(v);
+        }
+    }
+    __syncthreads();
+
+    auto runpv = [&](const unsigned short* Vb, size_t Vbs_, int KPB, int KK,
+                     int AOFF, int outoff) {
+        f32x4 pacc[13];
+#pragma unroll
+        for (int nt = 0; nt < 13; ++nt) pacc[nt] = (f32x4){0.f, 0.f, 0.f, 0.f};
+        const char* Bbase = (const char*)(Vb + (size_t)b * Vbs_);
+        auto stageB = [&](int kk) {
+            char* dst0 = &bbuf[kk & 1][0];
+#pragma unroll
+            for (int c = 0; c < 4; ++c) {
+                int idx = tid + c * 256;
+                if (idx < 832) {
+                    int lrow = idx >> 2, u = idx & 3;
+                    gas_void* src = (gas_void*)(Bbase + (size_t)lrow * (KPB * 2) +
+                                                kk * 64 + u * 16);
+                    __builtin_amdgcn_global_load_lds(src,
+                        (las_void*)(dst0 + (size_t)idx * 16), 16, 0, 0);
+                }
+            }
+        };
+        stageB(0);
+        __syncthreads();
+        for (int kk = 0; kk < KK; ++kk) {
+            if (kk + 1 < KK) stageB(kk + 1);
+            bf16x8 Af = *(const bf16x8*)&xsP[arow0 * 200 + AOFF + kk * 32 + kg * 8];
+            const char* bb = &bbuf[kk & 1][0];
+#pragma unroll
+            for (int nt = 0; nt < 13; ++nt) {
+                bf16x8 Bf = *(const bf16x8*)(bb + (nt * 16 + a) * 64 + kg * 16);
+                pacc[nt] = __builtin_amdgcn_mfma_f32_16x16x32_bf16(Af, Bf, pacc[nt], 0, 0, 0);
+            }
+            __syncthreads();
+        }
+#pragma unroll
+        for (int nt = 0; nt < 13; ++nt) {
+            int col = nt * 16 + a;
+#pragma unroll
+            for (int j = 0; j < 4; ++j) {
+                int row = mbase + j;
+                if (row < MROWS) {
+                    unsigned short h = (col < 196) ? f2bf(pacc[nt][j]) : (unsigned short)0;
+                    F[(size_t)row * 448 + outoff + col] = h;
+                }
+            }
+        }
+        {
+            int col = 208 + a;
+#pragma unroll
+            for (int j = 0; j < 4; ++j) {
+                int row = mbase + j;
+                if (row < MROWS) F[(size_t)row * 448 + outoff + col] = 0;
+            }
+        }
+    };
+    runpv(V1, (size_t)208 * 128, 128, 4, 0, 0);
+    runpv(V2, (size_t)208 * 64, 64, 2, 128, 224);
+}
+
 struct AG {
     const unsigned short* Ab; unsigned long ABS;
     const unsigned short* Bb; unsigned long BBS;
     const float* biasA; const float* biasB;
     const float* lnres; const float* res2;
-    unsigned short* p0; unsigned long p0rs, p0bs;
     float* feat; unsigned short* ftb; int cbase;
     int MROWS; int MTILES;
 };
 
-template <int KPA, int KPB, int KK, int EPI, int STAGEA, int NS>
+template <int KPA, int KPB, int KK, int NS>
 __global__ __launch_bounds__(256, 2) void k_agemm2(AG pa, AG pc, int split) {
     constexpr int KPS = KPA + 8;
-    __shared__ unsigned short xsA[STAGEA ? 64 * KPS : 64];
+    __shared__ unsigned short xsA[64];
     __shared__ char bbuf[2][208 * 64];
+    (void)xsA;
     const AG P = (blockIdx.x < split) ? pa : pc;
     const int bx = (blockIdx.x < split) ? blockIdx.x : blockIdx.x - split;
     const int tid = threadIdx.x, b = blockIdx.y;
@@ -698,17 +929,9 @@
     const int NT0 = (NS == 1) ? 0 : nh * 7;
     const int NTN = (NS == 1) ? 13 : ((nh == 0) ? 7 : 6);
     const int MROWS = P.MROWS, MTILES = P.MTILES;
+    (void)KPS;
 
     const unsigned short* Abase = P.Ab + (size_t)b * P.ABS;
-    if (STAGEA) {
-        const int rowu = KPA / 2;
-        for (int i = tid; i < 64 * rowu; i += 256) {
-            int r = i / rowu, cu = i - r * rowu;
-            int gr = mg * 64 + r; if (gr > MROWS - 1) gr = MROWS - 1;
-            unsigned int v = ((const unsigned int*)(Abase + (size_t)gr * KPA))[cu];
-            *(unsigned int*)&xsA[r * KPS + cu * 2] = v;
-        }
-    }
     const char* Bbase = (const char*)(P.Bb + (size_t)b * P.BBS);
     auto stageB = [&](int kk) {
         char* dst0 = &bbuf[kk & 1][0];
@@ -737,14 +960,8 @@
     __syncthreads();
     for (int kk = 0; kk < KK; ++kk) {
         if (kk + 1 < KK) stageB(kk + 1);
-        bf16x8 Af;
-        if (STAGEA) {
-            int arow = mt * 16 + a - mg * 64;
-            Af = *(const bf16x8*)&xsA[arow * KPS + kk * 32 + kg * 8];
-        } else {
-            int gr = mt * 16 + a; if (gr > MROWS - 1) gr = MROWS - 1;
-            Af = *(const bf16x8*)(Abase + (size_t)gr * KPA + kk * 32 + kg * 8);
-        }
+        int gr = mt * 16 + a; if (gr > MROWS - 1) gr = MROWS - 1;
+        bf16x8 Af = *(const bf16x8*)(Abase + (size_t)gr * KPA + kk * 32 + kg * 8);
         const char* bb = &bbuf[kk & 1][0];
 #pragma unroll
         for (int nt = 0; nt < 13; ++nt) {
@@ -757,163 +974,24 @@
     }
 
     const int mbase = mt * 16 + kg * 4;
-    if (EPI == 5) {
-#pragma unroll
-        for (int j = 0; j < 4; ++j) {
-            int row = mbase + j;
-            float mA = -3.4e38f, mB = -3.4e38f;
-#pragma unroll
-            for (int nt = 0; nt < 8; ++nt) mA = fmaxf(mA, acc[nt][j]);
-#pragma unroll
-            for (int nt = 8; nt < 13; ++nt) {
-                int col = nt * 16 + a;
-                float s = (col < 173) ? acc[nt][j] : -3.4e38f;
-                mB = fmaxf(mB, s);
-            }
-            for (int msk = 1; msk < 16; msk <<= 1) {
-                mA = fmaxf(mA, __shfl_xor(mA, msk));
-                mB = fmaxf(mB, __shfl_xor(mB, msk));
-            }
-            float eA[8], eB[5];
-            float sA = 0.f, sB = 0.f;
-#pragma unroll
-            for (int nt = 0; nt < 8; ++nt) { eA[nt] = expf(acc[nt][j] - mA); sA += eA[nt]; }
-#pragma unroll
-            for (int nt = 8; nt < 13; ++nt) {
-                int col = nt * 16 + a;
-                float v = (col < 173) ? expf(acc[nt][j] - mB) : 0.f;
-                eB[nt - 8] = v; sB += v;
-            }
-            for (int msk = 1; msk < 16; msk <<= 1) {
-                sA += __shfl_xor(sA, msk);
-                sB += __shfl_xor(sB, msk);
-            }
-            float iA = 1.f / sA, iB = 1.f / sB;
-            if (row < MROWS) {
-#pragma unroll
-                for (int nt = 0; nt < 12; ++nt) {
-                    int col = nt * 16 + a;
-                    float v = (nt < 8) ? eA[nt] * iA
-                                       : ((col < 173) ? eB[nt - 8] * iB : 0.f);
-                    P.p0[(size_t)b * P.p0bs + (size_t)row * P.p0rs + col] = f2bf(v);
-                }
-            }
-        }
-    } else {
-#pragma unroll
-        for (int nt = 0; nt < 13; ++nt) {
-            if (nt < NT0 || nt >= NT0 + NTN) continue;
-            int col = nt * 16 + a;
-            if (col < 196) {
-#pragma unroll
-                for (int j = 0; j < 4; ++j) {
-                    int row = mbase + j;
-                    if (row < MROWS) {
-                        size_t rr = ((size_t)b * MROWS + row) * 196 + col;
-                        float v = acc[nt][j] + P.biasA[col] + P.biasB[col] +
-                                  P.lnres[rr] + P.res2[rr];
-                        P.feat[((size_t)b * 173 + P.cbase + row) * 196 + col] = v;
-                        P.ftb[((size_t)(b * 208 + col)) * 192 + P.cbase + row] = f2bf(v);
-                    }
-                }
-            }
-        }
-    }
-}
-
-struct PVP { const unsigned short* P; unsigned long Pbs;
-             unsigned short* F; unsigned long Fbs; int MROWS; int MTILES; };
-
-__global__ __launch_bounds__(256, 2) void k_pv2(
-    PVP pa, PVP pc, int split,
-    const unsigned short* __restrict__ V1, unsigned long V1bs,
-    const unsigned short* __restrict__ V2, unsigned long V2bs) {
-    constexpr int KPS = 200;
-    __shared__ unsigned short xsA[64 * KPS];
-    __shared__ char bbuf[2][208 * 64];
-    const PVP P = (blockIdx.x < split) ? pa : pc;
-    const int bx = (blockIdx.x < split) ? blockIdx.x : blockIdx.x - split;
-    const int tid = threadIdx.x, b = blockIdx.y;
-    const int wv = tid >> 6, lane = tid & 63, a = lane & 15, kg = lane >> 4;
-    const int nh = bx % 2, mg = bx / 2;
-    const int NT0 = nh * 7, NTN = (nh == 0) ? 7 : 6;
-    const int MROWS = P.MROWS, MTILES = P.MTILES;
-
-    const unsigned short* Abase = P.P + (size_t)b * P.Pbs;
-    {
-        for (int i = tid; i < 64 * 96; i += 256) {
-            int r = i / 96, cu = i - r * 96;
-            int gr = mg * 64 + r; if (gr > MROWS - 1) gr = MROWS - 1;
-            unsigned int v = ((const unsigned int*)(Abase + (size_t)gr * 192))[cu];
-            *(unsigned int*)&xsA[r * KPS + cu * 2] = v;
-        }
-    }
-    int mt = mg * 4 + wv; if (mt > MTILES - 1) mt = MTILES - 1;
-    const int arow = mt * 16 + a - mg * 64;
-    const int mbase = mt * 16 + kg * 4;
-
-    auto run = [&](const unsigned short* Vb, size_t Vbs_, int KPB, int KK,
-                   int AOFFe, int outoff) {
-        f32x4 acc[13];
-#pragma unroll
-        for (int nt = 0; nt < 13; ++nt) acc[nt] = (f32x4){0.f, 0.f, 0.f, 0.f};
-        const char* Bbase = (const char*)(Vb + (size_t)b * Vbs_);
-        auto stageB = [&](int kk) {
-            char* dst0 = &bbuf[kk & 1][0];
-            const int cnt = NTN * 64;
-#pragma unroll
-            for (int c = 0; c < 4; ++c) {
-                int idx = tid + c * 256;
-                if (idx < cnt) {
-                    int lrow = idx >> 2, u = idx & 3;
-                    int grow = NT0 * 16 + lrow;
-                    gas_void* src = (gas_void*)(Bbase + (size_t)grow * (KPB * 2) +
-                                                kk * 64 + u * 16);
-                    __builtin_amdgcn_global_load_lds(src,
-                        (las_void*)(dst0 + (size_t)idx * 16), 16, 0, 0);
-                }
-            }
-        };
-        stageB(0);
-        __syncthreads();
-        for (int kk = 0; kk < KK; ++kk) {
-            if (kk + 1 < KK) stageB(kk + 1);
-            bf16x8 Af = *(const bf16x8*)&xsA[arow * KPS + AOFFe + kk * 32 + kg * 8];
-            const char* bb = &bbuf[kk & 1][0];
-#pragma unroll
-            for (int nt = 0; nt < 13; ++nt) {
-                if (nt >= NT0 && nt < NT0 + NTN) {
-                    bf16x8 Bf = *(const bf16x8*)(bb + ((nt - NT0) * 16 + a) * 64 + kg * 16);
-                    acc[nt] = __builtin_amdgcn_mfma_f32_16x16x32_bf16(Af, Bf, acc[nt], 0, 0, 0);
-                }
-            }
-            __syncthreads();
-        }
-#pragma unroll
-        for (int nt = 0; nt < 13; ++nt) {
-            if (nt < NT0 || nt >= NT0 + NTN) continue;
-            int col = nt * 16 + a;
+#pragma unroll
+    for (int nt = 0; nt < 13; ++nt) {
+        if (nt < NT0 || nt >= NT0 + NTN) continue;
+        int col = nt * 16 + a;
+        if (col < 196) {
 #pragma unroll
             for (int j = 0; j < 4; ++j) {
                 int row = mbase + j;
                 if (row < MROWS) {
-                    unsigned short h = (col < 196) ? f2bf(acc[nt][j]) : (unsigned short)0;
-                    P.F[(size_t)b * P.Fbs + (size_t)row * 448 + outoff + col] = h;
+                    size_t rr = ((size_t)b * MROWS + row) * 196 + col;
+                    float v = acc[nt][j] + P.biasA[col] + P.biasB[col] +
+                              P.lnres[rr] + P.res2[rr];
+                    P.feat[((size_t)b * 173 + P.cbase + row) * 196 + col] = v;
+                    P.ftb[((size_t)(b * 208 + col)) * 192 + P.cbase + row] = f2bf(v);
                 }
             }
         }
-        if (nh == 1) {
-            int col = 208 + a;
-#pragma unroll
-            for (int j = 0; j < 4; ++j) {
-                int row = mbase + j;
-                if (row < MROWS)
-                    P.F[(size_t)b * P.Fbs + (size_t)row * 448 + outoff + col] = 0;
-            }
-        }
-    };
-    run(V1, V1bs, 128, 4, 0, 0);
-    run(V2, V2bs, 64, 2, 128, 224);
+    }
 }
 
 template <int R, int ROWS, int KOFF, int TS>
@@ -1109,8 +1187,6 @@
     const size_t o_wcmf = o_wcm + 16896;
     const size_t o_ftb  = o_wcmf + 16896;
     const size_t o_tr   = o_ftb + 638976;
-    const size_t o_Pimg = o_tr;
-    const size_t o_Ptxt = o_tr + 393216;
     const size_t o_qtb  = o_tr;
     const size_t o_ps   = 10158208;
     const size_t o_xt1 = o_dd;
@@ -1130,8 +1206,6 @@
     unsigned short* wcatT = (unsigned short*)(W + o_wcT);
     unsigned short* Fimg = (unsigned short*)(W + o_Fimg);
     unsigned short* Ftxt = (unsigned short*)(W + o_Ftxt);
-    unsigned short* Pimg = (unsigned short*)(W + o_Pimg);
-    unsigned short* Ptxt = (unsigned short*)(W + o_Ptxt);
     unsigned short* ftb = (unsigned short*)(W + o_ftb);
     unsigned short* qtb = (unsigned short*)(W + o_qtb);
     unsigned short* feab = (unsigned short*)(W + o_qtb + 638976);
@@ -1160,10 +1234,9 @@
     k_bn_apply2<<<4096, 256, 0, stream>>>(W + o_B, W + o_ps + 8192, c1_g2, c1_be2,
                                           W + o_tr, fTb, nullptr, 128);
 
-    k_prep2<<<1658, 256, 0, stream>>>(cm_w, wcmb, cmf_w, wcmfb, gm1_w, gm1b,
-                                      (float4*)(W + o_ftb), gm2_w, e1_w, e2_w, W + o_wT);
-
-    k_cattext<<<392, 64, 0, stream>>>(oneHot, num, oh_w, oh_b, oh_g, oh_be,
+    k_prep2<<<1756, 256, 0, stream>>>(cm_w, wcmb, cmf_w, wcmfb, gm1_w, gm1b,
+                                      (float4*)(W + o_ftb), gm2_w, e1_w, e2_w, W + o_wT,
+                                      oneHot, num, oh_w, oh_b, oh_g, oh_be,
                                       nm_w, nm_b, nm_g, nm_be,
                                       W + o_toh, W + o_tnm, W + o_t1, W + o_tr + L);
 
@@ -1174,34 +1247,15 @@
                                                 W + o_d2, W + o_t1, gm2T, gm2_b,
                                                 W + o_t3);
 
-    k_bgemm<128, 8, 224, 7, 8, 2><<<dim3(4, 32), 256, 0, stream>>>(
-        tmpb, (size_t)128 * 224, gm1b, 0, gm1_b,
-        nullptr, nullptr, W + o_B, W + o_C);
-
-    k_prep3<<<936, 256, 0, stream>>>((float4*)(W + o_tqT), f1_w, f3_w, wcatI,
-                                     f4_w, f2_w, wcatT);
+    k_gcnfin<<<1064, 256, 0, stream>>>(tmpb, gm1b, gm1_b, W + o_B, W + o_C,
+                                       (float4*)(W + o_tqT), f1_w, f3_w, wcatI,
+                                       f4_w, f2_w, wcatT);
 
     k_lnlin_both<<<1504, 256, 0, stream>>>(W + o_C, ln1_g, ln1_b, e1T, e1_b, W + o_B,
                                            W + o_t3, ln2_g, ln2_b, e2T, e2_b, W + o_ln2,
                                            kcatb, iqTb, tqTb);
 
-    {
-        AG a{}, c{};
-        a.Ab = kcatb; a.ABS = 208 * 224; a.Bb = kcatb; a.BBS = 208 * 224;
-        a.p0 = Pimg; a.p0rs = 192; a.p0bs = (unsigned long)128 * 192;
-        a.MROWS = 128; a.MTILES = 8;
-        c = a;
-        c.Ab = kcatb + 128 * 224; c.p0 = Ptxt; c.p0bs = (unsigned long)48 * 192;
-        c.MROWS = 45; c.MTILES = 3;
-        k_agemm2<224, 224, 7, 5, 1, 1><<<dim3(3, 32), 256, 0, stream>>>(a, c, 2);
-    }
-
-    {
-        PVP a{Pimg, (unsigned long)128 * 192, Fimg, (unsigned long)128 * 448, 128, 8};
-        PVP c{Ptxt, (unsigned long)48 * 192, Ftxt, (unsigned long)48 * 448, 45, 3};
-        k_pv2<<<dim3(6, 32), 256, 0, stream>>>(a, c, 4, iqTb, (unsigned long)208 * 128,
-                                               tqTb, (unsigned long)208 * 64);
-    }
+    k_attn<<<96, 256, 0, stream>>>(kcatb, iqTb, tqTb, Fimg, Ftxt);
 
     {
         AG a{}, c{};
@@ -1212,7 +1266,7 @@
         c.Ab = Ftxt; c.ABS = (unsigned long)48 * 448; c.Bb = wcatT;
         c.biasA = f2_b; c.biasB = f4_b; c.lnres = W + o_ln2; c.res2 = W + o_t3;
         c.cbase = 128; c.MROWS = 45; c.MTILES = 3;
-        k_agemm2<448, 448, 14, 4, 0, 2><<<dim3(6, 32), 256, 0, stream>>>(a, c, 4);
+        k_agemm2<448, 448, 14, 2><<<dim3(6, 32), 256, 0, stream>>>(a, c, 4);
     }
 
     k_prep4<<<2592, 256, 0, stream>>>((float4*)(W + o_pbf), (float4*)(W + o_qtb));
```

Result: faster. 305.0 us (-4.1%).
